# Optimization experiments

Hardware: AMD Instinct MI355X
Metric: run time of the kernel (lower is better)

Reference implementation:

```python
import jax, jax.numpy as jnp
import numpy as np

B, L, E = 64, 256, 512
H = 1024          # hidden_size
N = 128           # memory_size
HS = 64           # head_size (memory width)
NH = 4            # NTM heads
OUT = 1024        # output_size
TNH = 4           # transformer nhead
IN_DIM = E + NH * HS          # 768
POD = H + NH * HS             # 1280


def ln(x, g, b, eps=1e-5):
    mu = x.mean(-1, keepdims=True)
    v = ((x - mu) ** 2).mean(-1, keepdims=True)
    return (x - mu) / jnp.sqrt(v + eps) * g + b


def setup_inputs() -> dict:
    key = jax.random.key(0)
    ks = iter(jax.random.split(key, 64))
    def w(shape, s=0.05):
        return jax.random.normal(next(ks), shape, jnp.float32) * s
    f32 = jnp.float32
    return dict(
        x_emb=jax.random.normal(next(ks), (B, L, E), f32),
        in_g=jnp.ones(IN_DIM, f32), in_b=jnp.zeros(IN_DIM, f32),
        W_ih=w((4 * H, IN_DIM)), W_hh=w((4 * H, H)),
        b_ih=jnp.zeros(4 * H, f32), b_hh=jnp.zeros(4 * H, f32),
        cn_g=jnp.ones(H, f32), cn_b=jnp.zeros(H, f32),
        W_rk=w((NH * HS, H)), b_rk=jnp.zeros(NH * HS, f32),
        W_wk=w((NH * HS, H)), b_wk=jnp.zeros(NH * HS, f32),
        W_ws=w((NH, H)), b_ws=jnp.zeros(NH, f32),
        W_ev=w((NH * HS, H)), b_ev=jnp.zeros(NH * HS, f32),
        attn_w=w((3 * HS, HS)), attn_b=jnp.zeros(3 * HS, f32),
        attn_ow=w((HS, HS)), attn_ob=jnp.zeros(HS, f32),
        l1_w=w((2 * HS, HS)), l1_b=jnp.zeros(2 * HS, f32),
        l2_w=w((HS, 2 * HS)), l2_b=jnp.zeros(HS, f32),
        tn1_g=jnp.ones(HS, f32), tn1_b=jnp.zeros(HS, f32),
        tn2_g=jnp.ones(HS, f32), tn2_b=jnp.zeros(HS, f32),
        rkn_g=jnp.ones(HS, f32), rkn_b=jnp.zeros(HS, f32),
        wkn_g=jnp.ones(HS, f32), wkn_b=jnp.zeros(HS, f32),
        mn_g=jnp.ones(HS, f32), mn_b=jnp.zeros(HS, f32),
        po_g=jnp.ones(POD, f32), po_b=jnp.zeros(POD, f32),
        W_proj=w((OUT, POD)), b_proj=jnp.zeros(OUT, f32),
    )


def reference(x_emb, in_g, in_b, W_ih, W_hh, b_ih, b_hh, cn_g, cn_b,
              W_rk, b_rk, W_wk, b_wk, W_ws, b_ws, W_ev, b_ev,
              attn_w, attn_b, attn_ow, attn_ob, l1_w, l1_b, l2_w, l2_b,
              tn1_g, tn1_b, tn2_g, tn2_b, rkn_g, rkn_b, wkn_g, wkn_b,
              mn_g, mn_b, po_g, po_b, W_proj, b_proj):
    Bc = x_emb.shape[0]
    dh = HS // TNH

    def tblock(mem):  # [B, N, HS], eval-mode (dropout = identity)
        qkv = mem @ attn_w.T + attn_b
        q, k, v = jnp.split(qkv, 3, axis=-1)
        q = q.reshape(Bc, N, TNH, dh)
        k = k.reshape(Bc, N, TNH, dh)
        v = v.reshape(Bc, N, TNH, dh)
        a = jax.nn.softmax(jnp.einsum('bqhd,bkhd->bhqk', q, k) / jnp.sqrt(jnp.float32(dh)), axis=-1)
        o = jnp.einsum('bhqk,bkhd->bqhd', a, v).reshape(Bc, N, HS)
        o = o @ attn_ow.T + attn_ob
        x = ln(mem + o, tn1_g, tn1_b)
        ff = jax.nn.gelu(x @ l1_w.T + l1_b, approximate=False) @ l2_w.T + l2_b
        return ln(x + ff, tn2_g, tn2_b)

    def step(carry, x_t):
        h, c, mem, rc = carry
        inp = ln(jnp.concatenate([x_t, rc.reshape(Bc, -1)], axis=-1), in_g, in_b)
        gates = inp @ W_ih.T + b_ih + h @ W_hh.T + b_hh  # torch gate order i,f,g,o
        i, f, g, o = jnp.split(gates, 4, axis=-1)
        c = jax.nn.sigmoid(f) * c + jax.nn.sigmoid(i) * jnp.tanh(g)
        h = jax.nn.sigmoid(o) * jnp.tanh(c)
        hn = ln(h, cn_g, cn_b)
        rk = (hn @ W_rk.T + b_rk).reshape(Bc, NH, HS)
        wk = (hn @ W_wk.T + b_wk).reshape(Bc, NH, HS)
        ws = jax.nn.sigmoid(hn @ W_ws.T + b_ws)                    # [B, NH]
        ev = jax.nn.sigmoid(hn @ W_ev.T + b_ev).reshape(Bc, NH, HS)
        # addressing
        mem = tblock(mem)
        mem_n = ln(mem, mn_g, mn_b)
        rk = ln(rk, rkn_g, rkn_b)
        wk = ln(wk, wkn_g, wkn_b)
        rw = jax.nn.softmax(jnp.einsum('bnk,bmk->bnm', rk, mem_n), axis=-1)
        rc = jnp.einsum('bnm,bmh->bnh', rw, mem)
        ww = jax.nn.softmax(jnp.einsum('bnk,bmk->bnm', wk, mem_n), axis=-1)
        erase = jnp.einsum('bnm,bnh->bmh', ww, ev)
        mem = mem * (1.0 - erase)
        add = jnp.einsum('bnm,bnh->bmh', ww, ws[..., None] * wk)
        mem = mem + add
        out = ln(jnp.concatenate([hn, rc.reshape(Bc, -1)], axis=-1), po_g, po_b)
        logits = out @ W_proj.T + b_proj
        return (h, c, mem, rc), logits

    h0 = jnp.zeros((Bc, H), x_emb.dtype)
    c0 = jnp.zeros((Bc, H), x_emb.dtype)
    mem0 = jnp.zeros((Bc, N, HS), x_emb.dtype)
    rc0 = jnp.zeros((Bc, NH, HS), x_emb.dtype)
    (h, c, mem, _), outs = jax.lax.scan(step, (h0, c0, mem0, rc0), jnp.swapaxes(x_emb, 0, 1))
    return jnp.swapaxes(outs, 0, 1), mem, (h[None], c[None])
```

## Files before the change

### kernel.cpp

```cpp
#include <hip/hip_runtime.h>
#include <math.h>

typedef short s8v __attribute__((ext_vector_type(8)));
typedef float f32x4 __attribute__((ext_vector_type(4)));

__device__ inline float sigm(float x) { return 1.0f / (1.0f + expf(-x)); }
__device__ inline float dot4(const float4 a, const float4 b) {
  return a.x*b.x + a.y*b.y + a.z*b.z + a.w*b.w;
}
__device__ inline float wsum(float v) {
#pragma unroll
  for (int o = 32; o > 0; o >>= 1) v += __shfl_xor(v, o, 64);
  return v;
}
__device__ inline short f2bf(float f) {
  unsigned int u = __float_as_uint(f);
  unsigned int r = u + 0x7FFFu + ((u >> 16) & 1u);
  return (short)(r >> 16);
}
__device__ inline float bf2f(short h) {
  return __uint_as_float(((unsigned int)(unsigned short)h) << 16);
}
__device__ inline void storesplit(float v, short* __restrict__ hi,
                                  short* __restrict__ lo, size_t idx) {
  short h = f2bf(v);
  hi[idx] = h;
  lo[idx] = f2bf(v - bf2f(h));
}

template<int LD, int KS>
__device__ __forceinline__ void gemm4(const short* __restrict__ A,
                                      const short* __restrict__ B,
                                      f32x4 acc[4], int lane) {
  int off = (lane & 15) * LD + ((lane >> 4) * 8);
#pragma unroll 4
  for (int kb = 0; kb < KS; kb++) {
    int ko = off + kb*32;
    s8v bb = *(const s8v*)(B + ko);
#pragma unroll
    for (int m = 0; m < 4; m++) {
      s8v aa = *(const s8v*)(A + ko + m*16*LD);
      acc[m] = __builtin_amdgcn_mfma_f32_16x16x32_bf16(aa, bb, acc[m], 0,0,0);
    }
  }
}

__global__ void kprep_g(const float* __restrict__ Wih, const float* __restrict__ Whh,
                        short* __restrict__ WgH, short* __restrict__ WgL) {
  int r = blockIdx.y, k = blockIdx.x*256 + threadIdx.x;
  if (k < 1792) {
    int jt = r >> 6, rr = r & 63, ul = rr >> 2, gi = rr & 3;
    int orow = gi*1024 + jt*16 + ul;
    float v = (k < 768) ? Wih[(size_t)orow*768 + k] : Whh[(size_t)orow*1024 + (k-768)];
    storesplit(v, WgH, WgL, (size_t)r*1792 + k);
  }
}
__global__ void kprep_p(const float* __restrict__ Wp, short* __restrict__ W) {
  int j = blockIdx.y, k = blockIdx.x*256 + threadIdx.x;
  W[(size_t)j*1280 + k] = f2bf(Wp[(size_t)j*1280 + k]);
}
__global__ void kprep_h(const float* __restrict__ Wrk, const float* __restrict__ Wwk,
                        const float* __restrict__ Wev, const float* __restrict__ Wws,
                        short* __restrict__ WhH, short* __restrict__ WhL) {
  int j = blockIdx.y, k = blockIdx.x*256 + threadIdx.x;
  float v;
  if (j < 256)      v = Wrk[(size_t)j*1024 + k];
  else if (j < 512) v = Wwk[(size_t)(j-256)*1024 + k];
  else if (j < 768) v = Wev[(size_t)(j-512)*1024 + k];
  else if (j < 772) v = Wws[(size_t)(j-768)*1024 + k];
  else v = 0.f;
  storesplit(v, WhH, WhL, (size_t)j*1024 + k);
}
__global__ void kprep_q(const float* __restrict__ aw, short* __restrict__ WH,
                        short* __restrict__ WL) {
  int i = blockIdx.x*64 + threadIdx.x;
  storesplit(aw[i], WH, WL, i);
}

__global__ __launch_bounds__(256) void k_prep0(
    const float* __restrict__ x_emb, const float* __restrict__ in_g,
    const float* __restrict__ in_b, short* __restrict__ inbH,
    short* __restrict__ inbL)
{
  __shared__ float rs[4], rq[4];
  int b = blockIdx.x, tid = threadIdx.x, lane = tid & 63, wid = tid >> 6;
  float v3[3]; float s = 0.f, sq = 0.f;
#pragma unroll
  for (int i = 0; i < 3; i++) {
    int k = tid + i * 256;
    float v = (k < 512) ? x_emb[(size_t)b * 256 * 512 + k] : 0.f;
    v3[i] = v; s += v; sq += v * v;
  }
  s = wsum(s); sq = wsum(sq);
  if (lane == 0) { rs[wid] = s; rq[wid] = sq; }
  __syncthreads();
  float ts = rs[0]+rs[1]+rs[2]+rs[3], tq = rq[0]+rq[1]+rq[2]+rq[3];
  float mu = ts / 768.f, var = tq / 768.f - mu * mu;
  float rstd = rsqrtf(var + 1e-5f);
#pragma unroll
  for (int i = 0; i < 3; i++) {
    int k = tid + i * 256;
    storesplit((v3[i] - mu) * rstd * in_g[k] + in_b[k], inbH, inbL, b*1792 + k);
  }
}

__global__ __launch_bounds__(256) void kA(
    const short* __restrict__ inbH, const short* __restrict__ inbL,
    short* __restrict__ inbHn, short* __restrict__ inbLn,
    const short* __restrict__ WgH, const short* __restrict__ WgL,
    const float* __restrict__ b_ih, const float* __restrict__ b_hh,
    float* __restrict__ cbuf, float* __restrict__ hbuf,
    float* __restrict__ hstat, float* __restrict__ gatesP,
    unsigned* __restrict__ tick,
    const short* __restrict__ membH, const short* __restrict__ membL,
    const short* __restrict__ WqH, const short* __restrict__ WqL,
    const float* __restrict__ attn_b,
    const short* __restrict__ pob16, const short* __restrict__ Wp16,
    const float* __restrict__ b_proj,
    float* __restrict__ qkv, float* __restrict__ outs, int t)
{
  __shared__ char poolA[40960];
  __shared__ unsigned sOld;
  int bid = blockIdx.x, tid = threadIdx.x, lane = tid & 63, w = tid >> 6;
  if (bid < 128) {
    if (t >= 256) return;
    short (*sT)[4][2560] = (short(*)[4][2560])poolA;
    int jt = bid & 63, kt = bid >> 6;
    int k0 = kt * 896;
    int srow = tid >> 2, scol = (tid & 3) * 8;
    const short* gAH = inbH + srow*1792 + k0 + scol;
    const short* gAL = inbL + srow*1792 + k0 + scol;
    const short* gBH = WgH + (size_t)(jt*64 + srow)*1792 + k0 + scol;
    const short* gBL = WgL + (size_t)(jt*64 + srow)*1792 + k0 + scol;
    int4 rAH = *(const int4*)gAH, rAL = *(const int4*)gAL;
    int4 rBH = *(const int4*)gBH, rBL = *(const int4*)gBL;
    *(int4*)&sT[0][0][srow*40 + scol] = rAH;
    *(int4*)&sT[0][1][srow*40 + scol] = rAL;
    *(int4*)&sT[0][2][srow*40 + scol] = rBH;
    *(int4*)&sT[0][3][srow*40 + scol] = rBL;
    f32x4 acc[4] = {};
    int arow = lane & 15, akk = (lane >> 4) * 8;
    for (int c = 0; c < 28; ++c) {
      int cur = c & 1;
      if (c < 27) {
        rAH = *(const int4*)(gAH + (c+1)*32);
        rAL = *(const int4*)(gAL + (c+1)*32);
        rBH = *(const int4*)(gBH + (c+1)*32);
        rBL = *(const int4*)(gBL + (c+1)*32);
      }
      __syncthreads();
      s8v bh = *(const s8v*)&sT[cur][2][(w*16 + arow)*40 + akk];
      s8v bl = *(const s8v*)&sT[cur][3][(w*16 + arow)*40 + akk];
#pragma unroll
      for (int ms = 0; ms < 4; ++ms) {
        s8v ah = *(const s8v*)&sT[cur][0][(arow + ms*16)*40 + akk];
        s8v al = *(const s8v*)&sT[cur][1][(arow + ms*16)*40 + akk];
        acc[ms] = __builtin_amdgcn_mfma_f32_16x16x32_bf16(ah, bh, acc[ms], 0,0,0);
        acc[ms] = __builtin_amdgcn_mfma_f32_16x16x32_bf16(al, bh, acc[ms], 0,0,0);
        acc[ms] = __builtin_amdgcn_mfma_f32_16x16x32_bf16(ah, bl, acc[ms], 0,0,0);
      }
      if (c < 27) {
        *(int4*)&sT[cur^1][0][srow*40 + scol] = rAH;
        *(int4*)&sT[cur^1][1][srow*40 + scol] = rAL;
        *(int4*)&sT[cur^1][2][srow*40 + scol] = rBH;
        *(int4*)&sT[cur^1][3][srow*40 + scol] = rBL;
      }
    }
    {
      float* gp = gatesP + (size_t)kt * 262144;
      int j = jt*64 + w*16 + (lane & 15);
#pragma unroll
      for (int ms = 0; ms < 4; ms++)
#pragma unroll
        for (int r = 0; r < 4; r++) {
          int b = ms*16 + (lane>>4)*4 + r;
          gp[b*4096 + j] = acc[ms][r];
        }
    }
    __syncthreads();
    if (tid == 0) {
      __threadfence();
      sOld = __hip_atomic_fetch_add(&tick[jt], 1u, __ATOMIC_ACQ_REL,
                                    __HIP_MEMORY_SCOPE_AGENT);
    }
    __syncthreads();
    if (!(sOld & 1u)) return;
    {
      const float* pp = gatesP + (size_t)(kt^1) * 262144;
      int j = jt*64 + w*16 + (lane & 15);
#pragma unroll
      for (int ms = 0; ms < 4; ms++)
#pragma unroll
        for (int r = 0; r < 4; r++) {
          int b = ms*16 + (lane>>4)*4 + r;
          acc[ms][r] += __hip_atomic_load(&pp[b*4096 + j], __ATOMIC_RELAXED,
                                          __HIP_MEMORY_SCOPE_AGENT);
        }
    }
    float* sC = (float*)poolA;
    float* sRed = (float*)(poolA + 17408);
    __syncthreads();
    {
      int rr = w*16 + (lane & 15);
#pragma unroll
      for (int ms = 0; ms < 4; ms++)
#pragma unroll
        for (int r = 0; r < 4; r++) {
          int b = ms*16 + (lane>>4)*4 + r;
          sC[b*68 + rr] = acc[ms][r];
        }
    }
    __syncthreads();
    {
      int b = tid & 63;
      float sh = 0.f, sh2 = 0.f;
#pragma unroll
      for (int q = 0; q < 4; q++) {
        int ul = (tid >> 6) + q*4;
        int u = jt*16 + ul;
        float gi_ = sC[b*68 + ul*4 + 0] + b_ih[u]        + b_hh[u];
        float gf  = sC[b*68 + ul*4 + 1] + b_ih[1024 + u] + b_hh[1024 + u];
        float gg  = sC[b*68 + ul*4 + 2] + b_ih[2048 + u] + b_hh[2048 + u];
        float go  = sC[b*68 + ul*4 + 3] + b_ih[3072 + u] + b_hh[3072 + u];
        float cn = sigm(gf)*cbuf[b*1024 + u] + sigm(gi_)*tanhf(gg);
        float hh = sigm(go)*tanhf(cn);
        cbuf[b*1024 + u] = cn;
        hbuf[b*1024 + u] = hh;
        storesplit(hh, inbHn, inbLn, b*1792 + 768 + u);
        sh += hh; sh2 += hh*hh;
      }
      sRed[(tid>>6)*64 + b] = sh;
      sRed[256 + (tid>>6)*64 + b] = sh2;
    }
    __syncthreads();
    if (tid < 64) {
      float s0 = sRed[tid]+sRed[64+tid]+sRed[128+tid]+sRed[192+tid];
      float s1 = sRed[256+tid]+sRed[320+tid]+sRed[384+tid]+sRed[448+tid];
      hstat[(tid*64 + jt)*2]     = s0;
      hstat[(tid*64 + jt)*2 + 1] = s1;
    }
  } else if (bid < 192) {
    if (t >= 256) return;
    int b = bid - 128;
    const short* Ah = membH + (size_t)b * 8192;
    const short* Al = membL + (size_t)b * 8192;
    int ao = (w*32 + (lane & 15)) * 64 + (lane >> 4) * 8;
    s8v ah00 = *(const s8v*)(Ah + ao);
    s8v ah01 = *(const s8v*)(Ah + ao + 32);
    s8v ah10 = *(const s8v*)(Ah + ao + 16*64);
    s8v ah11 = *(const s8v*)(Ah + ao + 16*64 + 32);
    s8v al00 = *(const s8v*)(Al + ao);
    s8v al01 = *(const s8v*)(Al + ao + 32);
    s8v al10 = *(const s8v*)(Al + ao + 16*64);
    s8v al11 = *(const s8v*)(Al + ao + 16*64 + 32);
    int bo = (lane & 15) * 64 + (lane >> 4) * 8;
    for (int n = 0; n < 12; n++) {
      s8v bh0 = *(const s8v*)(WqH + bo + n*1024);
      s8v bh1 = *(const s8v*)(WqH + bo + n*1024 + 32);
      s8v bl0 = *(const s8v*)(WqL + bo + n*1024);
      s8v bl1 = *(const s8v*)(WqL + bo + n*1024 + 32);
      f32x4 acc0 = {}, acc1 = {};
      acc0 = __builtin_amdgcn_mfma_f32_16x16x32_bf16(ah00, bh0, acc0, 0,0,0);
      acc0 = __builtin_amdgcn_mfma_f32_16x16x32_bf16(ah01, bh1, acc0, 0,0,0);
      acc0 = __builtin_amdgcn_mfma_f32_16x16x32_bf16(al00, bh0, acc0, 0,0,0);
      acc0 = __builtin_amdgcn_mfma_f32_16x16x32_bf16(al01, bh1, acc0, 0,0,0);
      acc0 = __builtin_amdgcn_mfma_f32_16x16x32_bf16(ah00, bl0, acc0, 0,0,0);
      acc0 = __builtin_amdgcn_mfma_f32_16x16x32_bf16(ah01, bl1, acc0, 0,0,0);
      acc1 = __builtin_amdgcn_mfma_f32_16x16x32_bf16(ah10, bh0, acc1, 0,0,0);
      acc1 = __builtin_amdgcn_mfma_f32_16x16x32_bf16(ah11, bh1, acc1, 0,0,0);
      acc1 = __builtin_amdgcn_mfma_f32_16x16x32_bf16(al10, bh0, acc1, 0,0,0);
      acc1 = __builtin_amdgcn_mfma_f32_16x16x32_bf16(al11, bh1, acc1, 0,0,0);
      acc1 = __builtin_amdgcn_mfma_f32_16x16x32_bf16(ah10, bl0, acc1, 0,0,0);
      acc1 = __builtin_amdgcn_mfma_f32_16x16x32_bf16(ah11, bl1, acc1, 0,0,0);
      int j = n*16 + (lane & 15);
      int ch = j >> 6, jj = j & 63;
      float bv = attn_b[j];
#pragma unroll
      for (int r = 0; r < 4; r++) {
        int m0 = w*32 + (lane>>4)*4 + r;
        qkv[((size_t)(b*3 + ch)*128 + m0)*64 + jj] = acc0[r] + bv;
        qkv[((size_t)(b*3 + ch)*128 + m0 + 16)*64 + jj] = acc1[r] + bv;
      }
    }
  } else {
    if (t == 0) return;
    int jt = bid - 192;
    f32x4 acc[4] = {};
    const short* B = Wp16 + (size_t)(jt*64 + w*16) * 1280;
    gemm4<1280, 40>(pob16, B, acc, lane);
    int j = jt*64 + w*16 + (lane & 15);
    float bv = b_proj[j];
#pragma unroll
    for (int ms = 0; ms < 4; ms++)
#pragma unroll
      for (int r = 0; r < 4; r++) {
        int b = ms*16 + (lane>>4)*4 + r;
        outs[((size_t)b*256 + (t-1))*1024 + j] = acc[ms][r] + bv;
      }
  }
}

__global__ __launch_bounds__(512) void kB(
    float* __restrict__ mem, const float* __restrict__ qkv,
    const float* __restrict__ attn_ow, const float* __restrict__ attn_ob,
    const float* __restrict__ l1w, const float* __restrict__ l1b,
    const float* __restrict__ l2w, const float* __restrict__ l2b,
    const float* __restrict__ tn1g, const float* __restrict__ tn1b,
    const float* __restrict__ tn2g, const float* __restrict__ tn2b,
    const float* __restrict__ hbuf, const float* __restrict__ hstat,
    const float* __restrict__ cn_g, const float* __restrict__ cn_b,
    const short* __restrict__ WhH, const short* __restrict__ WhL,
    float* __restrict__ hp)
{
  __shared__ float pool[35200];
  int bid = blockIdx.x, tid = threadIdx.x;
  int lane = tid & 63, wid = tid >> 6;
  if (bid < 52) {
    int kt = bid & 3, jt = bid >> 2;
    {
      int b2 = tid & 63, part = tid >> 6;
      float s0 = 0.f, s1 = 0.f;
#pragma unroll 4
      for (int m2 = 0; m2 < 8; m2++) {
        int jt2 = part*8 + m2;
        s0 += hstat[(b2*64 + jt2)*2];
        s1 += hstat[(b2*64 + jt2)*2 + 1];
      }
      pool[part*64 + b2] = s0;
      pool[512 + part*64 + b2] = s1;
    }
    __syncthreads();
    if (tid < 64) {
      float ts = 0.f, tq = 0.f;
#pragma unroll
      for (int p2 = 0; p2 < 8; p2++) {
        ts += pool[p2*64 + tid];
        tq += pool[512 + p2*64 + tid];
      }
      float mu = ts / 1024.f;
      pool[1024+tid] = mu;
      pool[1088+tid] = rsqrtf(tq/1024.f - mu*mu + 1e-5f);
    }
    __syncthreads();
    short* sAH = (short*)&pool[1152];
    short* sAL = sAH + 2560;
    int srow = tid >> 3, scol = (tid & 7) * 4;
    int arow = lane & 15, akk = (lane >> 4) * 8;
    f32x4 acc[4] = {};
    for (int c = 0; c < 8; ++c) {
      __syncthreads();
      {
        float mu = pool[1024 + srow], rsd = pool[1088 + srow];
        int kbase = kt*256 + c*32 + scol;
        const float* hpt = hbuf + srow*1024 + kbase;
#pragma unroll
        for (int i = 0; i < 4; i++) {
          float hnv = (hpt[i] - mu) * rsd * cn_g[kbase + i] + cn_b[kbase + i];
          short hh = f2bf(hnv);
          sAH[srow*40 + scol + i] = hh;
          sAL[srow*40 + scol + i] = f2bf(hnv - bf2f(hh));
        }
      }
      __syncthreads();
      if (wid < 4) {
        size_t bo = (size_t)(jt*64 + wid*16 + arow)*1024 + kt*256 + c*32 + akk;
        s8v bh = *(const s8v*)(WhH + bo);
        s8v bl = *(const s8v*)(WhL + bo);
#pragma unroll
        for (int ms = 0; ms < 4; ++ms) {
          s8v ah = *(const s8v*)&sAH[(arow + ms*16)*40 + akk];
          s8v al = *(const s8v*)&sAL[(arow + ms*16)*40 + akk];
          acc[ms] = __builtin_amdgcn_mfma_f32_16x16x32_bf16(ah, bh, acc[ms], 0,0,0);
          acc[ms] = __builtin_amdgcn_mfma_f32_16x16x32_bf16(al, bh, acc[ms], 0,0,0);
          acc[ms] = __builtin_amdgcn_mfma_f32_16x16x32_bf16(ah, bl, acc[ms], 0,0,0);
        }
      }
    }
    if (wid < 4) {
      int j = jt*64 + wid*16 + (lane & 15);
#pragma unroll
      for (int ms = 0; ms < 4; ms++)
#pragma unroll
        for (int r = 0; r < 4; r++) {
          int b2 = ms*16 + (lane>>4)*4 + r;
          hp[(size_t)kt*53248 + b2*832 + j] = acc[ms][r];
        }
    }
    return;
  }
  float* sK  = pool;
  float* sV  = pool + 8704;
  float* sX  = pool + 17408;
  float* sM  = pool + 19584;
  float* sO  = pool + 21760;
  float* sS  = pool + 23936;
  float* sRed= pool + 34176;
  int bb0 = bid - 52;
  int b = bb0 & 63, mt = bb0 >> 6;
  int m0 = mt * 32;
  const float* qb = qkv + (size_t)b*3*8192;
  for (int i = tid*4; i < 8192; i += 2048) {
    *(float4*)&sK[i] = *(const float4*)&qb[8192 + i];
    *(float4*)&sV[i] = *(const float4*)&qb[16384 + i];
  }
  {
    int i = tid*4;
    int m = i >> 6, s = i & 63;
    *(float4*)&sX[m*68+s] = *(const float4*)&qb[m0*64 + i];
    *(float4*)&sM[m*68+s] = *(const float4*)&mem[(size_t)b*8192 + m0*64 + i];
  }
  __syncthreads();
  int m = tid >> 4, hd = (tid >> 2) & 3, q = tid & 3;
  const float* qp = sX + m*68 + hd*16;
  float4 q0 = *(const float4*)(qp),   q1 = *(const float4*)(qp+4);
  float4 q2 = *(const float4*)(qp+8), q3 = *(const float4*)(qp+12);
  int kmb = q * 32;
  float mx = -1e30f;
#pragma unroll 4
  for (int kk = 0; kk < 32; kk++) {
    const float* kp = sK + (kmb+kk)*64 + hd*16;
    float sc = dot4(q0, *(const float4*)kp)     + dot4(q1, *(const float4*)(kp+4))
             + dot4(q2, *(const float4*)(kp+8)) + dot4(q3, *(const float4*)(kp+12));
    mx = fmaxf(mx, sc * 0.25f);
  }
  float4 o0 = {0,0,0,0}, o1 = {0,0,0,0}, o2 = {0,0,0,0}, o3 = {0,0,0,0};
  float sum = 0.f;
#pragma unroll 4
  for (int kk = 0; kk < 32; kk++) {
    const float* kp = sK + (kmb+kk)*64 + hd*16;
    float sc = dot4(q0, *(const float4*)kp)     + dot4(q1, *(const float4*)(kp+4))
             + dot4(q2, *(const float4*)(kp+8)) + dot4(q3, *(const float4*)(kp+12));
    float e = expf(sc * 0.25f - mx);
    sum += e;
    const float* vp = sV + (kmb+kk)*64 + hd*16;
    float4 v0 = *(const float4*)vp,     v1 = *(const float4*)(vp+4);
    float4 v2 = *(const float4*)(vp+8), v3 = *(const float4*)(vp+12);
    o0.x += e*v0.x; o0.y += e*v0.y; o0.z += e*v0.z; o0.w += e*v0.w;
    o1.x += e*v1.x; o1.y += e*v1.y; o1.z += e*v1.z; o1.w += e*v1.w;
    o2.x += e*v2.x; o2.y += e*v2.y; o2.z += e*v2.z; o2.w += e*v2.w;
    o3.x += e*v3.x; o3.y += e*v3.y; o3.z += e*v3.z; o3.w += e*v3.w;
  }
  {
    float* pp = sS + tid*20;
    *(float4*)&pp[0]  = o0; *(float4*)&pp[4]  = o1;
    *(float4*)&pp[8]  = o2; *(float4*)&pp[12] = o3;
    sRed[tid] = mx; sRed[512+tid] = sum;
  }
  __syncthreads();
  if (q == 0) {
    float m1 = sRed[tid+1], m2 = sRed[tid+2], m3 = sRed[tid+3];
    float M = fmaxf(fmaxf(mx, m1), fmaxf(m2, m3));
    float e0 = expf(mx - M), e1 = expf(m1 - M), e2 = expf(m2 - M), e3 = expf(m3 - M);
    float inv = 1.0f / (sum*e0 + sRed[512+tid+1]*e1 + sRed[512+tid+2]*e2
                        + sRed[512+tid+3]*e3);
    const float* p1 = sS + (tid+1)*20;
    const float* p2 = sS + (tid+2)*20;
    const float* p3 = sS + (tid+3)*20;
    float oo[16];
    *(float4*)&oo[0] = o0; *(float4*)&oo[4] = o1;
    *(float4*)&oo[8] = o2; *(float4*)&oo[12] = o3;
    float* op = sO + m*68 + hd*16;
#pragma unroll
    for (int d = 0; d < 16; d++)
      op[d] = (oo[d]*e0 + p1[d]*e1 + p2[d]*e2 + p3[d]*e3) * inv;
  }
  __syncthreads();
  for (int idx = tid; idx < 4096; idx += 512) {
    int j = idx >> 6, s = idx & 63;
    sS[j*68 + s] = attn_ow[idx];
  }
  __syncthreads();
  {
    int mm = tid >> 4, jset = tid & 15;
    float4 orow[16];
#pragma unroll
    for (int r = 0; r < 16; r++) orow[r] = *(const float4*)&sO[mm*68 + r*4];
#pragma unroll
    for (int i = 0; i < 4; i++) {
      int j = jset + 16*i;
      const float* wr = sS + j*68;
      float acc = attn_ob[j];
#pragma unroll
      for (int r = 0; r < 16; r++) acc += dot4(orow[r], *(const float4*)&wr[r*4]);
      sM[mm*68 + j] += acc;
    }
  }
  __syncthreads();
  for (int r = wid; r < 32; r += 8) {
    float v = sM[r*68 + lane];
    float ssum = wsum(v), ssq = wsum(v*v);
    float mu = ssum*(1.f/64), var = ssq*(1.f/64) - mu*mu;
    sX[r*68+lane] = (v - mu)*rsqrtf(var+1e-5f)*tn1g[lane] + tn1b[lane];
  }
  for (int idx = tid; idx < 8192; idx += 512) {
    int f = idx >> 6, s = idx & 63;
    sK[f*68 + s] = l1w[idx];
  }
  for (int idx = tid; idx < 8192; idx += 512) {
    int j = idx >> 7, s = idx & 127;
    sV[j*132 + s] = l2w[idx];
  }
  __syncthreads();
  {
    int mm = tid >> 4, fs = tid & 15;
    float4 xr[16];
#pragma unroll
    for (int r = 0; r < 16; r++) xr[r] = *(const float4*)&sX[mm*68 + r*4];
#pragma unroll 4
    for (int i = 0; i < 8; i++) {
      int f = fs + 16*i;
      const float* wr = sK + f*68;
      float acc = l1b[f];
#pragma unroll
      for (int r = 0; r < 16; r++) acc += dot4(xr[r], *(const float4*)&wr[r*4]);
      sS[mm*132 + f] = 0.5f*acc*(1.0f + erff(acc*0.70710678118654752f));
    }
  }
  __syncthreads();
  {
    int mm = tid >> 4, jset = tid & 15;
    float acc6[4];
#pragma unroll
    for (int i = 0; i < 4; i++) acc6[i] = sX[mm*68 + jset + 16*i] + l2b[jset + 16*i];
#pragma unroll
    for (int h = 0; h < 2; h++) {
      float4 fr[16];
#pragma unroll
      for (int r = 0; r < 16; r++) fr[r] = *(const float4*)&sS[mm*132 + h*64 + r*4];
#pragma unroll
      for (int i = 0; i < 4; i++) {
        int j = jset + 16*i;
        const float* wr = sV + j*132 + h*64;
        float a = 0.f;
#pragma unroll
        for (int r = 0; r < 16; r++) a += dot4(fr[r], *(const float4*)&wr[r*4]);
        acc6[i] += a;
      }
    }
#pragma unroll
    for (int i = 0; i < 4; i++) sO[mm*68 + jset + 16*i] = acc6[i];
  }
  __syncthreads();
  for (int r = wid; r < 32; r += 8) {
    float v = sO[r*68 + lane];
    float ssum = wsum(v), ssq = wsum(v*v);
    float mu = ssum*(1.f/64), var = ssq*(1.f/64) - mu*mu;
    mem[(size_t)b*8192 + (m0+r)*64 + lane] =
        (v - mu)*rsqrtf(var+1e-5f)*tn2g[lane] + tn2b[lane];
  }
}

__global__ __launch_bounds__(256) void kC(
    float* __restrict__ mem, short* __restrict__ membH, short* __restrict__ membL,
    const float* __restrict__ hp, const float* __restrict__ hstat,
    const float* __restrict__ hbuf,
    const float* __restrict__ b_rk, const float* __restrict__ b_wk,
    const float* __restrict__ b_ev, const float* __restrict__ b_ws,
    const float* __restrict__ rkn_g, const float* __restrict__ rkn_b,
    const float* __restrict__ wkn_g, const float* __restrict__ wkn_b,
    const float* __restrict__ cn_g, const float* __restrict__ cn_b,
    const float* __restrict__ mng, const float* __restrict__ mnb,
    const float* __restrict__ pog, const float* __restrict__ pob,
    const float* __restrict__ x_emb, const float* __restrict__ in_g,
    const float* __restrict__ in_b,
    short* __restrict__ inbHn, short* __restrict__ inbLn,
    short* __restrict__ pob16, int tnext)
{
  __shared__ float sMT[8192];
  __shared__ float sMN[128*65];
  __shared__ float sRk[256], sWk[256], sEv[256], sWs[4];
  __shared__ float sRw[512], sWw[512], sRc[256];
  __shared__ float rs[4], rq[4];
  __shared__ float sHst[2];
  int b = blockIdx.x, tid = threadIdx.x, lane = tid & 63, wid = tid >> 6;
  for (int i = tid*4; i < 8192; i += 1024)
    *(float4*)&sMT[i] = *(const float4*)&mem[(size_t)b*8192 + i];
  {
    const float* h0 = hp + (size_t)b*832;
    const float* h1 = hp + 53248 + (size_t)b*832;
    const float* h2 = hp + 2*53248 + (size_t)b*832;
    const float* h3 = hp + 3*53248 + (size_t)b*832;
    float v = h0[tid] + h1[tid] + h2[tid] + h3[tid] + b_rk[tid];
    float ssum = wsum(v), ssq = wsum(v*v);
    float mu = ssum*(1.f/64), var = ssq*(1.f/64) - mu*mu;
    sRk[tid] = (v - mu)*rsqrtf(var+1e-5f)*rkn_g[lane] + rkn_b[lane];
    v = h0[256+tid] + h1[256+tid] + h2[256+tid] + h3[256+tid] + b_wk[tid];
    ssum = wsum(v); ssq = wsum(v*v);
    mu = ssum*(1.f/64); var = ssq*(1.f/64) - mu*mu;
    sWk[tid] = (v - mu)*rsqrtf(var+1e-5f)*wkn_g[lane] + wkn_b[lane];
    sEv[tid] = sigm(h0[512+tid] + h1[512+tid] + h2[512+tid] + h3[512+tid] + b_ev[tid]);
    if (tid < 4)
      sWs[tid] = sigm(h0[768+tid] + h1[768+tid] + h2[768+tid] + h3[768+tid] + b_ws[tid]);
  }
  if (wid == 0) {
    float v0 = hstat[(b*64 + lane)*2], v1 = hstat[(b*64 + lane)*2 + 1];
    float s0 = wsum(v0), s1 = wsum(v1);
    if (lane == 0) {
      float mu = s0 / 1024.f;
      sHst[0] = mu;
      sHst[1] = rsqrtf(s1/1024.f - mu*mu + 1e-5f);
    }
  }
  __syncthreads();
  for (int r = wid; r < 128; r += 4) {
    float v = sMT[r*64 + lane];
    float ssum = wsum(v), ssq = wsum(v*v);
    float mu = ssum*(1.f/64), var = ssq*(1.f/64) - mu*mu;
    sMN[r*65 + lane] = (v - mu)*rsqrtf(var+1e-5f)*mng[lane] + mnb[lane];
  }
  __syncthreads();
#pragma unroll
  for (int q = 0; q < 4; q++) {
    int idx = tid + q*256;
    int which = idx >> 9;
    int n = (idx >> 7) & 3, m = idx & 127;
    const float* key = (which ? sWk : sRk) + n*64;
    const float* mr = sMN + m*65;
    float acc = 0.f;
#pragma unroll 8
    for (int k = 0; k < 64; k++) acc += key[k]*mr[k];
    (which ? sWw : sRw)[n*128 + m] = acc;
  }
  __syncthreads();
  for (int r = wid; r < 8; r += 4) {
    float* row = (r < 4) ? (sRw + r*128) : (sWw + (r-4)*128);
    float a0 = row[lane], a1 = row[lane+64];
    float mx = fmaxf(a0, a1);
#pragma unroll
    for (int o = 32; o > 0; o >>= 1) mx = fmaxf(mx, __shfl_xor(mx, o, 64));
    float e0 = expf(a0 - mx), e1 = expf(a1 - mx);
    float inv = 1.0f / wsum(e0 + e1);
    row[lane] = e0*inv; row[lane+64] = e1*inv;
  }
  __syncthreads();
  {
    int n = tid >> 6, s2 = tid & 63;
    float acc = 0.f;
    for (int mm = 0; mm < 128; mm++) acc += sRw[n*128 + mm] * sMT[mm*64 + s2];
    sRc[tid] = acc;
  }
  __syncthreads();
  for (int idx = tid; idx < 8192; idx += 256) {
    int mm = idx >> 6, s2 = idx & 63;
    float er = 0.f, ad = 0.f;
#pragma unroll
    for (int n = 0; n < 4; n++) {
      float w = sWw[n*128 + mm];
      er += w * sEv[n*64 + s2];
      ad += w * sWs[n] * sWk[n*64 + s2];
    }
    float val = sMT[idx]*(1.0f - er) + ad;
    mem[(size_t)b*8192 + idx] = val;
    storesplit(val, membH, membL, (size_t)b*8192 + idx);
  }
  float hmu = sHst[0], hrs = sHst[1];
  float v5[5]; float s = 0.f, sq = 0.f;
#pragma unroll
  for (int i = 0; i < 5; i++) {
    int k = tid + i*256;
    float v = (k < 1024)
      ? (hbuf[b*1024 + k] - hmu)*hrs*cn_g[k] + cn_b[k]
      : sRc[k-1024];
    v5[i] = v; s += v; sq += v*v;
  }
  s = wsum(s); sq = wsum(sq);
  if (lane == 0) { rs[wid] = s; rq[wid] = sq; }
  __syncthreads();
  {
    float ts = rs[0]+rs[1]+rs[2]+rs[3], tq = rq[0]+rq[1]+rq[2]+rq[3];
    float mu = ts/1280.f, var = tq/1280.f - mu*mu;
    float rstd = rsqrtf(var + 1e-5f);
#pragma unroll
    for (int i = 0; i < 5; i++) {
      int k = tid + i*256;
      pob16[b*1280 + k] = f2bf((v5[i] - mu)*rstd*pog[k] + pob[k]);
    }
  }
  if (tnext < 256) {
    __syncthreads();
    float v3[3]; float s2 = 0.f, q2 = 0.f;
#pragma unroll
    for (int i = 0; i < 3; i++) {
      int k = tid + i*256;
      float v = (k < 512) ? x_emb[((size_t)b*256 + tnext)*512 + k] : sRc[k-512];
      v3[i] = v; s2 += v; q2 += v*v;
    }
    s2 = wsum(s2); q2 = wsum(q2);
    if (lane == 0) { rs[wid] = s2; rq[wid] = q2; }
    __syncthreads();
    float ts = rs[0]+rs[1]+rs[2]+rs[3], tq = rq[0]+rq[1]+rq[2]+rq[3];
    float mu = ts/768.f, var = tq/768.f - mu*mu;
    float rstd = rsqrtf(var + 1e-5f);
#pragma unroll
    for (int i = 0; i < 3; i++) {
      int k = tid + i*256;
      storesplit((v3[i] - mu)*rstd*in_g[k] + in_b[k], inbHn, inbLn, b*1792 + k);
    }
  }
}

__global__ void k_final(const float* __restrict__ mem, const float* __restrict__ hbuf,
                        const float* __restrict__ cbuf, float* __restrict__ out)
{
  int i = blockIdx.x * 256 + threadIdx.x;
  if (i < 524288) out[16777216 + i] = mem[i];
  if (i < 65536) {
    out[17301504 + i] = hbuf[i];
    out[17367040 + i] = cbuf[i];
  }
}

extern "C" void kernel_launch(void* const* d_in, const int* in_sizes, int n_in,
                              void* d_out, int out_size, void* d_ws, size_t ws_size,
                              hipStream_t stream) {
  const float* x_emb  = (const float*)d_in[0];
  const float* in_g   = (const float*)d_in[1];
  const float* in_b   = (const float*)d_in[2];
  const float* W_ih   = (const float*)d_in[3];
  const float* W_hh   = (const float*)d_in[4];
  const float* b_ih   = (const float*)d_in[5];
  const float* b_hh   = (const float*)d_in[6];
  const float* cn_g   = (const float*)d_in[7];
  const float* cn_b   = (const float*)d_in[8];
  const float* W_rk   = (const float*)d_in[9];
  const float* b_rk   = (const float*)d_in[10];
  const float* W_wk   = (const float*)d_in[11];
  const float* b_wk   = (const float*)d_in[12];
  const float* W_ws   = (const float*)d_in[13];
  const float* b_ws   = (const float*)d_in[14];
  const float* W_ev   = (const float*)d_in[15];
  const float* b_ev   = (const float*)d_in[16];
  const float* attn_w = (const float*)d_in[17];
  const float* attn_b = (const float*)d_in[18];
  const float* attn_ow= (const float*)d_in[19];
  const float* attn_ob= (const float*)d_in[20];
  const float* l1_w   = (const float*)d_in[21];
  const float* l1_b   = (const float*)d_in[22];
  const float* l2_w   = (const float*)d_in[23];
  const float* l2_b   = (const float*)d_in[24];
  const float* tn1_g  = (const float*)d_in[25];
  const float* tn1_b  = (const float*)d_in[26];
  const float* tn2_g  = (const float*)d_in[27];
  const float* tn2_b  = (const float*)d_in[28];
  const float* rkn_g  = (const float*)d_in[29];
  const float* rkn_b  = (const float*)d_in[30];
  const float* wkn_g  = (const float*)d_in[31];
  const float* wkn_b  = (const float*)d_in[32];
  const float* mn_g   = (const float*)d_in[33];
  const float* mn_b   = (const float*)d_in[34];
  const float* po_g   = (const float*)d_in[35];
  const float* po_b   = (const float*)d_in[36];
  const float* W_proj = (const float*)d_in[37];
  const float* b_proj = (const float*)d_in[38];

  float* ws = (float*)d_ws;
  float* mem    = ws;
  float* cbuf   = ws + 524288;
  float* hbuf   = ws + 589824;
  float* gatesP = ws + 655360;
  float* hp     = ws + 1179648;
  float* hstat  = ws + 1392640;
  unsigned* tick = (unsigned*)(ws + 1400832);
  float* qkvb   = ws + 1400896;
  short* sb     = (short*)(ws + 2973760);
  short* inbH0 = sb;
  short* inbL0 = sb + 114688;
  short* inbH1 = sb + 229376;
  short* inbL1 = sb + 344064;
  short* membH = sb + 458752;
  short* membL = sb + 983040;
  short* pob16 = sb + 1507328;
  short* WgH   = sb + 1589248;
  short* WgL   = sb + 8929280;
  short* WhH   = sb + 16269312;
  short* WhL   = sb + 17121280;
  short* WqH   = sb + 17973248;
  short* WqL   = sb + 17985536;
  short* Wp16  = sb + 17997824;

  hipMemsetAsync(ws, 0, 655360 * sizeof(float), stream);
  hipMemsetAsync(tick, 0, 256, stream);
  hipMemsetAsync(sb, 0, 1507328 * sizeof(short), stream);

  kprep_g<<<dim3(7, 4096), 256, 0, stream>>>(W_ih, W_hh, WgH, WgL);
  kprep_p<<<dim3(5, 1024), 256, 0, stream>>>(W_proj, Wp16);
  kprep_h<<<dim3(4, 832), 256, 0, stream>>>(W_rk, W_wk, W_ev, W_ws, WhH, WhL);
  kprep_q<<<dim3(192), 64, 0, stream>>>(attn_w, WqH, WqL);
  k_prep0<<<64, 256, 0, stream>>>(x_emb, in_g, in_b, inbH0, inbL0);

  float* outs = (float*)d_out;
  short* bufsH[2] = {inbH0, inbH1};
  short* bufsL[2] = {inbL0, inbL1};
  for (int t = 0; t < 256; t++) {
    kA<<<208, 256, 0, stream>>>(bufsH[t&1], bufsL[t&1], bufsH[(t+1)&1], bufsL[(t+1)&1],
                                WgH, WgL, b_ih, b_hh, cbuf, hbuf, hstat, gatesP, tick,
                                membH, membL, WqH, WqL, attn_b,
                                pob16, Wp16, b_proj, qkvb, outs, t);
    kB<<<308, 512, 0, stream>>>(mem, qkvb, attn_ow, attn_ob,
                                l1_w, l1_b, l2_w, l2_b,
                                tn1_g, tn1_b, tn2_g, tn2_b,
                                hbuf, hstat, cn_g, cn_b, WhH, WhL, hp);
    kC<<<64, 256, 0, stream>>>(mem, membH, membL, hp, hstat, hbuf,
                               b_rk, b_wk, b_ev, b_ws,
                               rkn_g, rkn_b, wkn_g, wkn_b, cn_g, cn_b,
                               mn_g, mn_b, po_g, po_b,
                               x_emb, in_g, in_b,
                               bufsH[(t+1)&1], bufsL[(t+1)&1], pob16, t+1);
  }
  kA<<<208, 256, 0, stream>>>(bufsH[0], bufsL[0], bufsH[1], bufsL[1],
                              WgH, WgL, b_ih, b_hh, cbuf, hbuf, hstat, gatesP, tick,
                              membH, membL, WqH, WqL, attn_b,
                              pob16, Wp16, b_proj, qkvb, outs, 256);
  k_final<<<2048, 256, 0, stream>>>(mem, hbuf, cbuf, (float*)d_out);
}
```

Measured before the change: 27.37 ms.

## Restructure step pipeline from three kernels to two, fusing transformer block into LSTM kernel

The per-timestep schedule now uses two kernels instead of three. The transformer block over memory moves into spare blocks of the LSTM/projection kernel, and the QKV projection moves into the addressing kernel, which computes it from the freshly updated memory held in shared memory. The LSTM gate GEMM now splits K across two halves of a 512-thread block and reduces through shared memory, replacing the cross-block atomic tick and global partial buffer. Head projections now read fp32 weights directly in kC rather than the pre-split bf16 copies. This removes one launch per step and the global membH/membL round trip, at the cost of heavier, more register-hungry fused blocks and fewer blocks doing the gate GEMM.

```diff
diff --git a/kernel.cpp b/kernel.cpp
--- a/kernel.cpp
+++ b/kernel.cpp
@@ -59,18 +59,6 @@
   int j = blockIdx.y, k = blockIdx.x*256 + threadIdx.x;
   W[(size_t)j*1280 + k] = f2bf(Wp[(size_t)j*1280 + k]);
 }
-__global__ void kprep_h(const float* __restrict__ Wrk, const float* __restrict__ Wwk,
-                        const float* __restrict__ Wev, const float* __restrict__ Wws,
-                        short* __restrict__ WhH, short* __restrict__ WhL) {
-  int j = blockIdx.y, k = blockIdx.x*256 + threadIdx.x;
-  float v;
-  if (j < 256)      v = Wrk[(size_t)j*1024 + k];
-  else if (j < 512) v = Wwk[(size_t)(j-256)*1024 + k];
-  else if (j < 768) v = Wev[(size_t)(j-512)*1024 + k];
-  else if (j < 772) v = Wws[(size_t)(j-768)*1024 + k];
-  else v = 0.f;
-  storesplit(v, WhH, WhL, (size_t)j*1024 + k);
-}
 __global__ void kprep_q(const float* __restrict__ aw, short* __restrict__ WH,
                         short* __restrict__ WL) {
   int i = blockIdx.x*64 + threadIdx.x;
@@ -104,30 +92,44 @@
   }
 }
 
-__global__ __launch_bounds__(256) void kA(
+__global__ __launch_bounds__(256) void k_prepq0(
+    const float* __restrict__ attn_b, float* __restrict__ qkv)
+{
+  int b = blockIdx.x, tid = threadIdx.x;
+  for (int i = tid; i < 24576; i += 256) {
+    int ch = i >> 13, j = i & 63;
+    qkv[(size_t)b*24576 + i] = attn_b[ch*64 + j];
+  }
+}
+
+__global__ __launch_bounds__(512) void kA(
     const short* __restrict__ inbH, const short* __restrict__ inbL,
     short* __restrict__ inbHn, short* __restrict__ inbLn,
     const short* __restrict__ WgH, const short* __restrict__ WgL,
     const float* __restrict__ b_ih, const float* __restrict__ b_hh,
     float* __restrict__ cbuf, float* __restrict__ hbuf,
-    float* __restrict__ hstat, float* __restrict__ gatesP,
-    unsigned* __restrict__ tick,
-    const short* __restrict__ membH, const short* __restrict__ membL,
-    const short* __restrict__ WqH, const short* __restrict__ WqL,
-    const float* __restrict__ attn_b,
+    float* __restrict__ hstat,
+    const float* __restrict__ qkv, float* __restrict__ mem,
+    const float* __restrict__ attn_ow, const float* __restrict__ attn_ob,
+    const float* __restrict__ l1w, const float* __restrict__ l1b,
+    const float* __restrict__ l2w, const float* __restrict__ l2b,
+    const float* __restrict__ tn1g, const float* __restrict__ tn1b,
+    const float* __restrict__ tn2g, const float* __restrict__ tn2b,
     const short* __restrict__ pob16, const short* __restrict__ Wp16,
-    const float* __restrict__ b_proj,
-    float* __restrict__ qkv, float* __restrict__ outs, int t)
+    const float* __restrict__ b_proj, float* __restrict__ outs, int t)
 {
-  __shared__ char poolA[40960];
-  __shared__ unsigned sOld;
-  int bid = blockIdx.x, tid = threadIdx.x, lane = tid & 63, w = tid >> 6;
-  if (bid < 128) {
+  __shared__ float pool[35200];
+  int bid = blockIdx.x, tid = threadIdx.x;
+  int lane = tid & 63;
+  if (bid < 64) {
     if (t >= 256) return;
-    short (*sT)[4][2560] = (short(*)[4][2560])poolA;
-    int jt = bid & 63, kt = bid >> 6;
+    int jt = bid;
+    int kt = tid >> 8;
+    int tl = tid & 255;
+    int w4 = (tid >> 6) & 3;
+    short (*sT)[4][2560] = (short(*)[4][2560])((char*)pool + kt*40960);
     int k0 = kt * 896;
-    int srow = tid >> 2, scol = (tid & 3) * 8;
+    int srow = tl >> 2, scol = (tl & 3) * 8;
     const short* gAH = inbH + srow*1792 + k0 + scol;
     const short* gAL = inbL + srow*1792 + k0 + scol;
     const short* gBH = WgH + (size_t)(jt*64 + srow)*1792 + k0 + scol;
@@ -149,8 +151,8 @@
         rBL = *(const int4*)(gBL + (c+1)*32);
       }
       __syncthreads();
-      s8v bh = *(const s8v*)&sT[cur][2][(w*16 + arow)*40 + akk];
-      s8v bl = *(const s8v*)&sT[cur][3][(w*16 + arow)*40 + akk];
+      s8v bh = *(const s8v*)&sT[cur][2][(w4*16 + arow)*40 + akk];
+      s8v bl = *(const s8v*)&sT[cur][3][(w4*16 + arow)*40 + akk];
 #pragma unroll
       for (int ms = 0; ms < 4; ++ms) {
         s8v ah = *(const s8v*)&sT[cur][0][(arow + ms*16)*40 + akk];
@@ -166,62 +168,32 @@
         *(int4*)&sT[cur^1][3][srow*40 + scol] = rBL;
       }
     }
+    __syncthreads();
+    float* sC = pool;
+    float* sRed = pool + 8704;
     {
-      float* gp = gatesP + (size_t)kt * 262144;
-      int j = jt*64 + w*16 + (lane & 15);
+      float* sCk = sC + kt*4352;
+      int rr = w4*16 + (lane & 15);
 #pragma unroll
       for (int ms = 0; ms < 4; ms++)
 #pragma unroll
         for (int r = 0; r < 4; r++) {
           int b = ms*16 + (lane>>4)*4 + r;
-          gp[b*4096 + j] = acc[ms][r];
+          sCk[b*68 + rr] = acc[ms][r];
         }
     }
-    __syncthreads();
-    if (tid == 0) {
-      __threadfence();
-      sOld = __hip_atomic_fetch_add(&tick[jt], 1u, __ATOMIC_ACQ_REL,
-                                    __HIP_MEMORY_SCOPE_AGENT);
-    }
-    __syncthreads();
-    if (!(sOld & 1u)) return;
-    {
-      const float* pp = gatesP + (size_t)(kt^1) * 262144;
-      int j = jt*64 + w*16 + (lane & 15);
-#pragma unroll
-      for (int ms = 0; ms < 4; ms++)
-#pragma unroll
-        for (int r = 0; r < 4; r++) {
-          int b = ms*16 + (lane>>4)*4 + r;
-          acc[ms][r] += __hip_atomic_load(&pp[b*4096 + j], __ATOMIC_RELAXED,
-                                          __HIP_MEMORY_SCOPE_AGENT);
-        }
-    }
-    float* sC = (float*)poolA;
-    float* sRed = (float*)(poolA + 17408);
     __syncthreads();
     {
-      int rr = w*16 + (lane & 15);
-#pragma unroll
-      for (int ms = 0; ms < 4; ms++)
-#pragma unroll
-        for (int r = 0; r < 4; r++) {
-          int b = ms*16 + (lane>>4)*4 + r;
-          sC[b*68 + rr] = acc[ms][r];
-        }
-    }
-    __syncthreads();
-    {
-      int b = tid & 63;
+      int b = tid & 63, ug = tid >> 6;
       float sh = 0.f, sh2 = 0.f;
 #pragma unroll
-      for (int q = 0; q < 4; q++) {
-        int ul = (tid >> 6) + q*4;
+      for (int q = 0; q < 2; q++) {
+        int ul = ug*2 + q;
         int u = jt*16 + ul;
-        float gi_ = sC[b*68 + ul*4 + 0] + b_ih[u]        + b_hh[u];
-        float gf  = sC[b*68 + ul*4 + 1] + b_ih[1024 + u] + b_hh[1024 + u];
-        float gg  = sC[b*68 + ul*4 + 2] + b_ih[2048 + u] + b_hh[2048 + u];
-        float go  = sC[b*68 + ul*4 + 3] + b_ih[3072 + u] + b_hh[3072 + u];
+        float gi_ = sC[b*68 + ul*4 + 0] + sC[4352 + b*68 + ul*4 + 0] + b_ih[u]        + b_hh[u];
+        float gf  = sC[b*68 + ul*4 + 1] + sC[4352 + b*68 + ul*4 + 1] + b_ih[1024 + u] + b_hh[1024 + u];
+        float gg  = sC[b*68 + ul*4 + 2] + sC[4352 + b*68 + ul*4 + 2] + b_ih[2048 + u] + b_hh[2048 + u];
+        float go  = sC[b*68 + ul*4 + 3] + sC[4352 + b*68 + ul*4 + 3] + b_ih[3072 + u] + b_hh[3072 + u];
         float cn = sigm(gf)*cbuf[b*1024 + u] + sigm(gi_)*tanhf(gg);
         float hh = sigm(go)*tanhf(cn);
         cbuf[b*1024 + u] = cn;
@@ -229,66 +201,191 @@
         storesplit(hh, inbHn, inbLn, b*1792 + 768 + u);
         sh += hh; sh2 += hh*hh;
       }
-      sRed[(tid>>6)*64 + b] = sh;
-      sRed[256 + (tid>>6)*64 + b] = sh2;
+      sRed[ug*64 + b] = sh;
+      sRed[512 + ug*64 + b] = sh2;
     }
     __syncthreads();
     if (tid < 64) {
-      float s0 = sRed[tid]+sRed[64+tid]+sRed[128+tid]+sRed[192+tid];
-      float s1 = sRed[256+tid]+sRed[320+tid]+sRed[384+tid]+sRed[448+tid];
+      float s0 = 0.f, s1 = 0.f;
+#pragma unroll
+      for (int p = 0; p < 8; p++) { s0 += sRed[p*64 + tid]; s1 += sRed[512 + p*64 + tid]; }
       hstat[(tid*64 + jt)*2]     = s0;
       hstat[(tid*64 + jt)*2 + 1] = s1;
     }
   } else if (bid < 192) {
     if (t >= 256) return;
-    int b = bid - 128;
-    const short* Ah = membH + (size_t)b * 8192;
-    const short* Al = membL + (size_t)b * 8192;
-    int ao = (w*32 + (lane & 15)) * 64 + (lane >> 4) * 8;
-    s8v ah00 = *(const s8v*)(Ah + ao);
-    s8v ah01 = *(const s8v*)(Ah + ao + 32);
-    s8v ah10 = *(const s8v*)(Ah + ao + 16*64);
-    s8v ah11 = *(const s8v*)(Ah + ao + 16*64 + 32);
-    s8v al00 = *(const s8v*)(Al + ao);
-    s8v al01 = *(const s8v*)(Al + ao + 32);
-    s8v al10 = *(const s8v*)(Al + ao + 16*64);
-    s8v al11 = *(const s8v*)(Al + ao + 16*64 + 32);
-    int bo = (lane & 15) * 64 + (lane >> 4) * 8;
-    for (int n = 0; n < 12; n++) {
-      s8v bh0 = *(const s8v*)(WqH + bo + n*1024);
-      s8v bh1 = *(const s8v*)(WqH + bo + n*1024 + 32);
-      s8v bl0 = *(const s8v*)(WqL + bo + n*1024);
-      s8v bl1 = *(const s8v*)(WqL + bo + n*1024 + 32);
-      f32x4 acc0 = {}, acc1 = {};
-      acc0 = __builtin_amdgcn_mfma_f32_16x16x32_bf16(ah00, bh0, acc0, 0,0,0);
-      acc0 = __builtin_amdgcn_mfma_f32_16x16x32_bf16(ah01, bh1, acc0, 0,0,0);
-      acc0 = __builtin_amdgcn_mfma_f32_16x16x32_bf16(al00, bh0, acc0, 0,0,0);
-      acc0 = __builtin_amdgcn_mfma_f32_16x16x32_bf16(al01, bh1, acc0, 0,0,0);
-      acc0 = __builtin_amdgcn_mfma_f32_16x16x32_bf16(ah00, bl0, acc0, 0,0,0);
-      acc0 = __builtin_amdgcn_mfma_f32_16x16x32_bf16(ah01, bl1, acc0, 0,0,0);
-      acc1 = __builtin_amdgcn_mfma_f32_16x16x32_bf16(ah10, bh0, acc1, 0,0,0);
-      acc1 = __builtin_amdgcn_mfma_f32_16x16x32_bf16(ah11, bh1, acc1, 0,0,0);
-      acc1 = __builtin_amdgcn_mfma_f32_16x16x32_bf16(al10, bh0, acc1, 0,0,0);
-      acc1 = __builtin_amdgcn_mfma_f32_16x16x32_bf16(al11, bh1, acc1, 0,0,0);
-      acc1 = __builtin_amdgcn_mfma_f32_16x16x32_bf16(ah10, bl0, acc1, 0,0,0);
-      acc1 = __builtin_amdgcn_mfma_f32_16x16x32_bf16(ah11, bl1, acc1, 0,0,0);
-      int j = n*16 + (lane & 15);
-      int ch = j >> 6, jj = j & 63;
-      float bv = attn_b[j];
-#pragma unroll
-      for (int r = 0; r < 4; r++) {
-        int m0 = w*32 + (lane>>4)*4 + r;
-        qkv[((size_t)(b*3 + ch)*128 + m0)*64 + jj] = acc0[r] + bv;
-        qkv[((size_t)(b*3 + ch)*128 + m0 + 16)*64 + jj] = acc1[r] + bv;
-      }
+    float* sK  = pool;
+    float* sV  = pool + 8704;
+    float* sX  = pool + 17408;
+    float* sM  = pool + 19584;
+    float* sO  = pool + 21760;
+    float* sS  = pool + 23936;
+    float* sRed= pool + 34176;
+    int pb = bid - 64;
+    int b = pb & 63, pr = pb >> 6;
+    int wid = tid >> 6;
+    const float* qb = qkv + (size_t)b*3*8192;
+    for (int it = 0; it < 2; ++it) {
+      int m0 = (pr*2 + it) * 32;
+      for (int i = tid*4; i < 8192; i += 2048) {
+        *(float4*)&sK[i] = *(const float4*)&qb[8192 + i];
+        *(float4*)&sV[i] = *(const float4*)&qb[16384 + i];
+      }
+      {
+        int i = tid*4;
+        int m = i >> 6, s = i & 63;
+        *(float4*)&sX[m*68+s] = *(const float4*)&qb[m0*64 + i];
+        *(float4*)&sM[m*68+s] = *(const float4*)&mem[(size_t)b*8192 + m0*64 + i];
+      }
+      __syncthreads();
+      int m = tid >> 4, hd = (tid >> 2) & 3, q = tid & 3;
+      const float* qp = sX + m*68 + hd*16;
+      float4 q0 = *(const float4*)(qp),   q1 = *(const float4*)(qp+4);
+      float4 q2 = *(const float4*)(qp+8), q3 = *(const float4*)(qp+12);
+      int kmb = q * 32;
+      float mx = -1e30f;
+#pragma unroll 4
+      for (int kk = 0; kk < 32; kk++) {
+        const float* kp = sK + (kmb+kk)*64 + hd*16;
+        float sc = dot4(q0, *(const float4*)kp)     + dot4(q1, *(const float4*)(kp+4))
+                 + dot4(q2, *(const float4*)(kp+8)) + dot4(q3, *(const float4*)(kp+12));
+        mx = fmaxf(mx, sc * 0.25f);
+      }
+      float4 o0 = {0,0,0,0}, o1 = {0,0,0,0}, o2 = {0,0,0,0}, o3 = {0,0,0,0};
+      float sum = 0.f;
+#pragma unroll 4
+      for (int kk = 0; kk < 32; kk++) {
+        const float* kp = sK + (kmb+kk)*64 + hd*16;
+        float sc = dot4(q0, *(const float4*)kp)     + dot4(q1, *(const float4*)(kp+4))
+                 + dot4(q2, *(const float4*)(kp+8)) + dot4(q3, *(const float4*)(kp+12));
+        float e = expf(sc * 0.25f - mx);
+        sum += e;
+        const float* vp = sV + (kmb+kk)*64 + hd*16;
+        float4 v0 = *(const float4*)vp,     v1 = *(const float4*)(vp+4);
+        float4 v2 = *(const float4*)(vp+8), v3 = *(const float4*)(vp+12);
+        o0.x += e*v0.x; o0.y += e*v0.y; o0.z += e*v0.z; o0.w += e*v0.w;
+        o1.x += e*v1.x; o1.y += e*v1.y; o1.z += e*v1.z; o1.w += e*v1.w;
+        o2.x += e*v2.x; o2.y += e*v2.y; o2.z += e*v2.z; o2.w += e*v2.w;
+        o3.x += e*v3.x; o3.y += e*v3.y; o3.z += e*v3.z; o3.w += e*v3.w;
+      }
+      {
+        float* pp = sS + tid*20;
+        *(float4*)&pp[0]  = o0; *(float4*)&pp[4]  = o1;
+        *(float4*)&pp[8]  = o2; *(float4*)&pp[12] = o3;
+        sRed[tid] = mx; sRed[512+tid] = sum;
+      }
+      __syncthreads();
+      if (q == 0) {
+        float m1 = sRed[tid+1], m2 = sRed[tid+2], m3 = sRed[tid+3];
+        float M = fmaxf(fmaxf(mx, m1), fmaxf(m2, m3));
+        float e0 = expf(mx - M), e1 = expf(m1 - M), e2 = expf(m2 - M), e3 = expf(m3 - M);
+        float inv = 1.0f / (sum*e0 + sRed[512+tid+1]*e1 + sRed[512+tid+2]*e2
+                            + sRed[512+tid+3]*e3);
+        const float* p1 = sS + (tid+1)*20;
+        const float* p2 = sS + (tid+2)*20;
+        const float* p3 = sS + (tid+3)*20;
+        float oo[16];
+        *(float4*)&oo[0] = o0; *(float4*)&oo[4] = o1;
+        *(float4*)&oo[8] = o2; *(float4*)&oo[12] = o3;
+        float* op = sO + m*68 + hd*16;
+#pragma unroll
+        for (int d = 0; d < 16; d++)
+          op[d] = (oo[d]*e0 + p1[d]*e1 + p2[d]*e2 + p3[d]*e3) * inv;
+      }
+      __syncthreads();
+      for (int idx = tid; idx < 4096; idx += 512) {
+        int j = idx >> 6, s = idx & 63;
+        sS[j*68 + s] = attn_ow[idx];
+      }
+      __syncthreads();
+      {
+        int mm = tid >> 4, jset = tid & 15;
+        float4 orow[16];
+#pragma unroll
+        for (int r = 0; r < 16; r++) orow[r] = *(const float4*)&sO[mm*68 + r*4];
+#pragma unroll
+        for (int i = 0; i < 4; i++) {
+          int j = jset + 16*i;
+          const float* wr = sS + j*68;
+          float acc = attn_ob[j];
+#pragma unroll
+          for (int r = 0; r < 16; r++) acc += dot4(orow[r], *(const float4*)&wr[r*4]);
+          sM[mm*68 + j] += acc;
+        }
+      }
+      __syncthreads();
+      for (int r = wid; r < 32; r += 8) {
+        float v = sM[r*68 + lane];
+        float ssum = wsum(v), ssq = wsum(v*v);
+        float mu = ssum*(1.f/64), var = ssq*(1.f/64) - mu*mu;
+        sX[r*68+lane] = (v - mu)*rsqrtf(var+1e-5f)*tn1g[lane] + tn1b[lane];
+      }
+      for (int idx = tid; idx < 8192; idx += 512) {
+        int f = idx >> 6, s = idx & 63;
+        sK[f*68 + s] = l1w[idx];
+      }
+      for (int idx = tid; idx < 8192; idx += 512) {
+        int j = idx >> 7, s = idx & 127;
+        sV[j*132 + s] = l2w[idx];
+      }
+      __syncthreads();
+      {
+        int mm = tid >> 4, fs = tid & 15;
+        float4 xr[16];
+#pragma unroll
+        for (int r = 0; r < 16; r++) xr[r] = *(const float4*)&sX[mm*68 + r*4];
+#pragma unroll 4
+        for (int i = 0; i < 8; i++) {
+          int f = fs + 16*i;
+          const float* wr = sK + f*68;
+          float acc = l1b[f];
+#pragma unroll
+          for (int r = 0; r < 16; r++) acc += dot4(xr[r], *(const float4*)&wr[r*4]);
+          sS[mm*132 + f] = 0.5f*acc*(1.0f + erff(acc*0.70710678118654752f));
+        }
+      }
+      __syncthreads();
+      {
+        int mm = tid >> 4, jset = tid & 15;
+        float acc6[4];
+#pragma unroll
+        for (int i = 0; i < 4; i++) acc6[i] = sX[mm*68 + jset + 16*i] + l2b[jset + 16*i];
+#pragma unroll
+        for (int h = 0; h < 2; h++) {
+          float4 fr[16];
+#pragma unroll
+          for (int r = 0; r < 16; r++) fr[r] = *(const float4*)&sS[mm*132 + h*64 + r*4];
+#pragma unroll
+          for (int i = 0; i < 4; i++) {
+            int j = jset + 16*i;
+            const float* wr = sV + j*132 + h*64;
+            float a = 0.f;
+#pragma unroll
+            for (int r = 0; r < 16; r++) a += dot4(fr[r], *(const float4*)&wr[r*4]);
+            acc6[i] += a;
+          }
+        }
+#pragma unroll
+        for (int i = 0; i < 4; i++) sO[mm*68 + jset + 16*i] = acc6[i];
+      }
+      __syncthreads();
+      for (int r = wid; r < 32; r += 8) {
+        float v = sO[r*68 + lane];
+        float ssum = wsum(v), ssq = wsum(v*v);
+        float mu = ssum*(1.f/64), var = ssq*(1.f/64) - mu*mu;
+        mem[(size_t)b*8192 + (m0+r)*64 + lane] =
+            (v - mu)*rsqrtf(var+1e-5f)*tn2g[lane] + tn2b[lane];
+      }
+      __syncthreads();
     }
   } else {
     if (t == 0) return;
     int jt = bid - 192;
+    int w = tid >> 6;
     f32x4 acc[4] = {};
-    const short* B = Wp16 + (size_t)(jt*64 + w*16) * 1280;
+    const short* B = Wp16 + (size_t)(jt*128 + w*16) * 1280;
     gemm4<1280, 40>(pob16, B, acc, lane);
-    int j = jt*64 + w*16 + (lane & 15);
+    int j = jt*128 + w*16 + (lane & 15);
     float bv = b_proj[j];
 #pragma unroll
     for (int ms = 0; ms < 4; ms++)
@@ -300,299 +397,46 @@
   }
 }
 
-__global__ __launch_bounds__(512) void kB(
-    float* __restrict__ mem, const float* __restrict__ qkv,
-    const float* __restrict__ attn_ow, const float* __restrict__ attn_ob,
-    const float* __restrict__ l1w, const float* __restrict__ l1b,
-    const float* __restrict__ l2w, const float* __restrict__ l2b,
-    const float* __restrict__ tn1g, const float* __restrict__ tn1b,
-    const float* __restrict__ tn2g, const float* __restrict__ tn2b,
-    const float* __restrict__ hbuf, const float* __restrict__ hstat,
+__global__ __launch_bounds__(512) void kC(
+    float* __restrict__ mem, const float* __restrict__ hstat,
+    const float* __restrict__ hbuf,
     const float* __restrict__ cn_g, const float* __restrict__ cn_b,
-    const short* __restrict__ WhH, const short* __restrict__ WhL,
-    float* __restrict__ hp)
-{
-  __shared__ float pool[35200];
-  int bid = blockIdx.x, tid = threadIdx.x;
-  int lane = tid & 63, wid = tid >> 6;
-  if (bid < 52) {
-    int kt = bid & 3, jt = bid >> 2;
-    {
-      int b2 = tid & 63, part = tid >> 6;
-      float s0 = 0.f, s1 = 0.f;
-#pragma unroll 4
-      for (int m2 = 0; m2 < 8; m2++) {
-        int jt2 = part*8 + m2;
-        s0 += hstat[(b2*64 + jt2)*2];
-        s1 += hstat[(b2*64 + jt2)*2 + 1];
-      }
-      pool[part*64 + b2] = s0;
-      pool[512 + part*64 + b2] = s1;
-    }
-    __syncthreads();
-    if (tid < 64) {
-      float ts = 0.f, tq = 0.f;
-#pragma unroll
-      for (int p2 = 0; p2 < 8; p2++) {
-        ts += pool[p2*64 + tid];
-        tq += pool[512 + p2*64 + tid];
-      }
-      float mu = ts / 1024.f;
-      pool[1024+tid] = mu;
-      pool[1088+tid] = rsqrtf(tq/1024.f - mu*mu + 1e-5f);
-    }
-    __syncthreads();
-    short* sAH = (short*)&pool[1152];
-    short* sAL = sAH + 2560;
-    int srow = tid >> 3, scol = (tid & 7) * 4;
-    int arow = lane & 15, akk = (lane >> 4) * 8;
-    f32x4 acc[4] = {};
-    for (int c = 0; c < 8; ++c) {
-      __syncthreads();
-      {
-        float mu = pool[1024 + srow], rsd = pool[1088 + srow];
-        int kbase = kt*256 + c*32 + scol;
-        const float* hpt = hbuf + srow*1024 + kbase;
-#pragma unroll
-        for (int i = 0; i < 4; i++) {
-          float hnv = (hpt[i] - mu) * rsd * cn_g[kbase + i] + cn_b[kbase + i];
-          short hh = f2bf(hnv);
-          sAH[srow*40 + scol + i] = hh;
-          sAL[srow*40 + scol + i] = f2bf(hnv - bf2f(hh));
-        }
-      }
-      __syncthreads();
-      if (wid < 4) {
-        size_t bo = (size_t)(jt*64 + wid*16 + arow)*1024 + kt*256 + c*32 + akk;
-        s8v bh = *(const s8v*)(WhH + bo);
-        s8v bl = *(const s8v*)(WhL + bo);
-#pragma unroll
-        for (int ms = 0; ms < 4; ++ms) {
-          s8v ah = *(const s8v*)&sAH[(arow + ms*16)*40 + akk];
-          s8v al = *(const s8v*)&sAL[(arow + ms*16)*40 + akk];
-          acc[ms] = __builtin_amdgcn_mfma_f32_16x16x32_bf16(ah, bh, acc[ms], 0,0,0);
-          acc[ms] = __builtin_amdgcn_mfma_f32_16x16x32_bf16(al, bh, acc[ms], 0,0,0);
-          acc[ms] = __builtin_amdgcn_mfma_f32_16x16x32_bf16(ah, bl, acc[ms], 0,0,0);
-        }
-      }
-    }
-    if (wid < 4) {
-      int j = jt*64 + wid*16 + (lane & 15);
-#pragma unroll
-      for (int ms = 0; ms < 4; ms++)
-#pragma unroll
-        for (int r = 0; r < 4; r++) {
-          int b2 = ms*16 + (lane>>4)*4 + r;
-          hp[(size_t)kt*53248 + b2*832 + j] = acc[ms][r];
-        }
-    }
-    return;
-  }
-  float* sK  = pool;
-  float* sV  = pool + 8704;
-  float* sX  = pool + 17408;
-  float* sM  = pool + 19584;
-  float* sO  = pool + 21760;
-  float* sS  = pool + 23936;
-  float* sRed= pool + 34176;
-  int bb0 = bid - 52;
-  int b = bb0 & 63, mt = bb0 >> 6;
-  int m0 = mt * 32;
-  const float* qb = qkv + (size_t)b*3*8192;
-  for (int i = tid*4; i < 8192; i += 2048) {
-    *(float4*)&sK[i] = *(const float4*)&qb[8192 + i];
-    *(float4*)&sV[i] = *(const float4*)&qb[16384 + i];
-  }
-  {
-    int i = tid*4;
-    int m = i >> 6, s = i & 63;
-    *(float4*)&sX[m*68+s] = *(const float4*)&qb[m0*64 + i];
-    *(float4*)&sM[m*68+s] = *(const float4*)&mem[(size_t)b*8192 + m0*64 + i];
-  }
-  __syncthreads();
-  int m = tid >> 4, hd = (tid >> 2) & 3, q = tid & 3;
-  const float* qp = sX + m*68 + hd*16;
-  float4 q0 = *(const float4*)(qp),   q1 = *(const float4*)(qp+4);
-  float4 q2 = *(const float4*)(qp+8), q3 = *(const float4*)(qp+12);
-  int kmb = q * 32;
-  float mx = -1e30f;
-#pragma unroll 4
-  for (int kk = 0; kk < 32; kk++) {
-    const float* kp = sK + (kmb+kk)*64 + hd*16;
-    float sc = dot4(q0, *(const float4*)kp)     + dot4(q1, *(const float4*)(kp+4))
-             + dot4(q2, *(const float4*)(kp+8)) + dot4(q3, *(const float4*)(kp+12));
-    mx = fmaxf(mx, sc * 0.25f);
-  }
-  float4 o0 = {0,0,0,0}, o1 = {0,0,0,0}, o2 = {0,0,0,0}, o3 = {0,0,0,0};
-  float sum = 0.f;
-#pragma unroll 4
-  for (int kk = 0; kk < 32; kk++) {
-    const float* kp = sK + (kmb+kk)*64 + hd*16;
-    float sc = dot4(q0, *(const float4*)kp)     + dot4(q1, *(const float4*)(kp+4))
-             + dot4(q2, *(const float4*)(kp+8)) + dot4(q3, *(const float4*)(kp+12));
-    float e = expf(sc * 0.25f - mx);
-    sum += e;
-    const float* vp = sV + (kmb+kk)*64 + hd*16;
-    float4 v0 = *(const float4*)vp,     v1 = *(const float4*)(vp+4);
-    float4 v2 = *(const float4*)(vp+8), v3 = *(const float4*)(vp+12);
-    o0.x += e*v0.x; o0.y += e*v0.y; o0.z += e*v0.z; o0.w += e*v0.w;
-    o1.x += e*v1.x; o1.y += e*v1.y; o1.z += e*v1.z; o1.w += e*v1.w;
-    o2.x += e*v2.x; o2.y += e*v2.y; o2.z += e*v2.z; o2.w += e*v2.w;
-    o3.x += e*v3.x; o3.y += e*v3.y; o3.z += e*v3.z; o3.w += e*v3.w;
-  }
-  {
-    float* pp = sS + tid*20;
-    *(float4*)&pp[0]  = o0; *(float4*)&pp[4]  = o1;
-    *(float4*)&pp[8]  = o2; *(float4*)&pp[12] = o3;
-    sRed[tid] = mx; sRed[512+tid] = sum;
-  }
-  __syncthreads();
-  if (q == 0) {
-    float m1 = sRed[tid+1], m2 = sRed[tid+2], m3 = sRed[tid+3];
-    float M = fmaxf(fmaxf(mx, m1), fmaxf(m2, m3));
-    float e0 = expf(mx - M), e1 = expf(m1 - M), e2 = expf(m2 - M), e3 = expf(m3 - M);
-    float inv = 1.0f / (sum*e0 + sRed[512+tid+1]*e1 + sRed[512+tid+2]*e2
-                        + sRed[512+tid+3]*e3);
-    const float* p1 = sS + (tid+1)*20;
-    const float* p2 = sS + (tid+2)*20;
-    const float* p3 = sS + (tid+3)*20;
-    float oo[16];
-    *(float4*)&oo[0] = o0; *(float4*)&oo[4] = o1;
-    *(float4*)&oo[8] = o2; *(float4*)&oo[12] = o3;
-    float* op = sO + m*68 + hd*16;
-#pragma unroll
-    for (int d = 0; d < 16; d++)
-      op[d] = (oo[d]*e0 + p1[d]*e1 + p2[d]*e2 + p3[d]*e3) * inv;
-  }
-  __syncthreads();
-  for (int idx = tid; idx < 4096; idx += 512) {
-    int j = idx >> 6, s = idx & 63;
-    sS[j*68 + s] = attn_ow[idx];
-  }
-  __syncthreads();
-  {
-    int mm = tid >> 4, jset = tid & 15;
-    float4 orow[16];
-#pragma unroll
-    for (int r = 0; r < 16; r++) orow[r] = *(const float4*)&sO[mm*68 + r*4];
-#pragma unroll
-    for (int i = 0; i < 4; i++) {
-      int j = jset + 16*i;
-      const float* wr = sS + j*68;
-      float acc = attn_ob[j];
-#pragma unroll
-      for (int r = 0; r < 16; r++) acc += dot4(orow[r], *(const float4*)&wr[r*4]);
-      sM[mm*68 + j] += acc;
-    }
-  }
-  __syncthreads();
-  for (int r = wid; r < 32; r += 8) {
-    float v = sM[r*68 + lane];
-    float ssum = wsum(v), ssq = wsum(v*v);
-    float mu = ssum*(1.f/64), var = ssq*(1.f/64) - mu*mu;
-    sX[r*68+lane] = (v - mu)*rsqrtf(var+1e-5f)*tn1g[lane] + tn1b[lane];
-  }
-  for (int idx = tid; idx < 8192; idx += 512) {
-    int f = idx >> 6, s = idx & 63;
-    sK[f*68 + s] = l1w[idx];
-  }
-  for (int idx = tid; idx < 8192; idx += 512) {
-    int j = idx >> 7, s = idx & 127;
-    sV[j*132 + s] = l2w[idx];
-  }
-  __syncthreads();
-  {
-    int mm = tid >> 4, fs = tid & 15;
-    float4 xr[16];
-#pragma unroll
-    for (int r = 0; r < 16; r++) xr[r] = *(const float4*)&sX[mm*68 + r*4];
-#pragma unroll 4
-    for (int i = 0; i < 8; i++) {
-      int f = fs + 16*i;
-      const float* wr = sK + f*68;
-      float acc = l1b[f];
-#pragma unroll
-      for (int r = 0; r < 16; r++) acc += dot4(xr[r], *(const float4*)&wr[r*4]);
-      sS[mm*132 + f] = 0.5f*acc*(1.0f + erff(acc*0.70710678118654752f));
-    }
-  }
-  __syncthreads();
-  {
-    int mm = tid >> 4, jset = tid & 15;
-    float acc6[4];
-#pragma unroll
-    for (int i = 0; i < 4; i++) acc6[i] = sX[mm*68 + jset + 16*i] + l2b[jset + 16*i];
-#pragma unroll
-    for (int h = 0; h < 2; h++) {
-      float4 fr[16];
-#pragma unroll
-      for (int r = 0; r < 16; r++) fr[r] = *(const float4*)&sS[mm*132 + h*64 + r*4];
-#pragma unroll
-      for (int i = 0; i < 4; i++) {
-        int j = jset + 16*i;
-        const float* wr = sV + j*132 + h*64;
-        float a = 0.f;
-#pragma unroll
-        for (int r = 0; r < 16; r++) a += dot4(fr[r], *(const float4*)&wr[r*4]);
-        acc6[i] += a;
-      }
-    }
-#pragma unroll
-    for (int i = 0; i < 4; i++) sO[mm*68 + jset + 16*i] = acc6[i];
-  }
-  __syncthreads();
-  for (int r = wid; r < 32; r += 8) {
-    float v = sO[r*68 + lane];
-    float ssum = wsum(v), ssq = wsum(v*v);
-    float mu = ssum*(1.f/64), var = ssq*(1.f/64) - mu*mu;
-    mem[(size_t)b*8192 + (m0+r)*64 + lane] =
-        (v - mu)*rsqrtf(var+1e-5f)*tn2g[lane] + tn2b[lane];
-  }
-}
-
-__global__ __launch_bounds__(256) void kC(
-    float* __restrict__ mem, short* __restrict__ membH, short* __restrict__ membL,
-    const float* __restrict__ hp, const float* __restrict__ hstat,
-    const float* __restrict__ hbuf,
+    const float* __restrict__ W_rk, const float* __restrict__ W_wk,
+    const float* __restrict__ W_ev, const float* __restrict__ W_ws,
     const float* __restrict__ b_rk, const float* __restrict__ b_wk,
     const float* __restrict__ b_ev, const float* __restrict__ b_ws,
     const float* __restrict__ rkn_g, const float* __restrict__ rkn_b,
     const float* __restrict__ wkn_g, const float* __restrict__ wkn_b,
-    const float* __restrict__ cn_g, const float* __restrict__ cn_b,
     const float* __restrict__ mng, const float* __restrict__ mnb,
     const float* __restrict__ pog, const float* __restrict__ pob,
     const float* __restrict__ x_emb, const float* __restrict__ in_g,
     const float* __restrict__ in_b,
+    const short* __restrict__ WqH, const short* __restrict__ WqL,
+    const float* __restrict__ attn_b,
+    float* __restrict__ qkv,
     short* __restrict__ inbHn, short* __restrict__ inbLn,
     short* __restrict__ pob16, int tnext)
 {
-  __shared__ float sMT[8192];
-  __shared__ float sMN[128*65];
-  __shared__ float sRk[256], sWk[256], sEv[256], sWs[4];
-  __shared__ float sRw[512], sWw[512], sRc[256];
-  __shared__ float rs[4], rq[4];
-  __shared__ float sHst[2];
-  int b = blockIdx.x, tid = threadIdx.x, lane = tid & 63, wid = tid >> 6;
-  for (int i = tid*4; i < 8192; i += 1024)
+  __shared__ float P[20960];
+  float* sMT  = P;
+  float* sMN  = P + 8192;
+  float* sHn  = P + 16512;
+  float* sHOut= P + 17536;
+  float* sRk  = P + 18368;
+  float* sWk  = P + 18624;
+  float* sEv  = P + 18880;
+  float* sWs  = P + 19136;
+  float* sRw  = P + 19140;
+  float* sWw  = P + 19652;
+  float* sRc  = P + 20164;
+  float* sRcP = P + 20420;
+  float* rs   = P + 20932;
+  float* rq   = P + 20940;
+  float* sHst = P + 20948;
+  int b = blockIdx.x, tid = threadIdx.x, lane = tid & 63, wv = tid >> 6;
+  for (int i = tid*4; i < 8192; i += 2048)
     *(float4*)&sMT[i] = *(const float4*)&mem[(size_t)b*8192 + i];
-  {
-    const float* h0 = hp + (size_t)b*832;
-    const float* h1 = hp + 53248 + (size_t)b*832;
-    const float* h2 = hp + 2*53248 + (size_t)b*832;
-    const float* h3 = hp + 3*53248 + (size_t)b*832;
-    float v = h0[tid] + h1[tid] + h2[tid] + h3[tid] + b_rk[tid];
-    float ssum = wsum(v), ssq = wsum(v*v);
-    float mu = ssum*(1.f/64), var = ssq*(1.f/64) - mu*mu;
-    sRk[tid] = (v - mu)*rsqrtf(var+1e-5f)*rkn_g[lane] + rkn_b[lane];
-    v = h0[256+tid] + h1[256+tid] + h2[256+tid] + h3[256+tid] + b_wk[tid];
-    ssum = wsum(v); ssq = wsum(v*v);
-    mu = ssum*(1.f/64); var = ssq*(1.f/64) - mu*mu;
-    sWk[tid] = (v - mu)*rsqrtf(var+1e-5f)*wkn_g[lane] + wkn_b[lane];
-    sEv[tid] = sigm(h0[512+tid] + h1[512+tid] + h2[512+tid] + h3[512+tid] + b_ev[tid]);
-    if (tid < 4)
-      sWs[tid] = sigm(h0[768+tid] + h1[768+tid] + h2[768+tid] + h3[768+tid] + b_ws[tid]);
-  }
-  if (wid == 0) {
+  if (wv == 0) {
     float v0 = hstat[(b*64 + lane)*2], v1 = hstat[(b*64 + lane)*2 + 1];
     float s0 = wsum(v0), s1 = wsum(v1);
     if (lane == 0) {
@@ -602,16 +446,49 @@
     }
   }
   __syncthreads();
-  for (int r = wid; r < 128; r += 4) {
+  {
+    float mu = sHst[0], rstd = sHst[1];
+    for (int u = tid; u < 1024; u += 512)
+      sHn[u] = (hbuf[b*1024 + u] - mu)*rstd*cn_g[u] + cn_b[u];
+  }
+  for (int r = wv; r < 128; r += 8) {
     float v = sMT[r*64 + lane];
     float ssum = wsum(v), ssq = wsum(v*v);
     float mu = ssum*(1.f/64), var = ssq*(1.f/64) - mu*mu;
     sMN[r*65 + lane] = (v - mu)*rsqrtf(var+1e-5f)*mng[lane] + mnb[lane];
   }
   __syncthreads();
-#pragma unroll
-  for (int q = 0; q < 4; q++) {
-    int idx = tid + q*256;
+  for (int r = wv; r < 772; r += 8) {
+    const float* wr;
+    if (r < 256)      wr = W_rk + (size_t)r*1024;
+    else if (r < 512) wr = W_wk + (size_t)(r-256)*1024;
+    else if (r < 768) wr = W_ev + (size_t)(r-512)*1024;
+    else              wr = W_ws + (size_t)(r-768)*1024;
+    float acc = 0.f;
+#pragma unroll
+    for (int i = 0; i < 16; i++) acc += wr[lane + 64*i] * sHn[lane + 64*i];
+    acc = wsum(acc);
+    if (lane == 0) sHOut[r] = acc;
+  }
+  __syncthreads();
+  if (wv < 4) {
+    float v = sHOut[wv*64 + lane] + b_rk[wv*64 + lane];
+    float ssum = wsum(v), ssq = wsum(v*v);
+    float mu = ssum*(1.f/64), var = ssq*(1.f/64) - mu*mu;
+    sRk[wv*64 + lane] = (v - mu)*rsqrtf(var+1e-5f)*rkn_g[lane] + rkn_b[lane];
+  } else {
+    int n = wv - 4;
+    float v = sHOut[256 + n*64 + lane] + b_wk[n*64 + lane];
+    float ssum = wsum(v), ssq = wsum(v*v);
+    float mu = ssum*(1.f/64), var = ssq*(1.f/64) - mu*mu;
+    sWk[n*64 + lane] = (v - mu)*rsqrtf(var+1e-5f)*wkn_g[lane] + wkn_b[lane];
+  }
+  if (tid < 256) sEv[tid] = sigm(sHOut[512 + tid] + b_ev[tid]);
+  if (tid >= 256 && tid < 260) sWs[tid-256] = sigm(sHOut[768 + (tid-256)] + b_ws[tid-256]);
+  __syncthreads();
+#pragma unroll
+  for (int q = 0; q < 2; q++) {
+    int idx = tid + q*512;
     int which = idx >> 9;
     int n = (idx >> 7) & 3, m = idx & 127;
     const float* key = (which ? sWk : sRk) + n*64;
@@ -622,8 +499,8 @@
     (which ? sWw : sRw)[n*128 + m] = acc;
   }
   __syncthreads();
-  for (int r = wid; r < 8; r += 4) {
-    float* row = (r < 4) ? (sRw + r*128) : (sWw + (r-4)*128);
+  {
+    float* row = (wv < 4) ? (sRw + wv*128) : (sWw + (wv-4)*128);
     float a0 = row[lane], a1 = row[lane+64];
     float mx = fmaxf(a0, a1);
 #pragma unroll
@@ -634,13 +511,15 @@
   }
   __syncthreads();
   {
-    int n = tid >> 6, s2 = tid & 63;
+    int idx = tid & 255, h2 = tid >> 8;
+    int n = idx >> 6, s2 = idx & 63;
     float acc = 0.f;
-    for (int mm = 0; mm < 128; mm++) acc += sRw[n*128 + mm] * sMT[mm*64 + s2];
-    sRc[tid] = acc;
-  }
-  __syncthreads();
-  for (int idx = tid; idx < 8192; idx += 256) {
+    for (int mm = h2*64; mm < h2*64 + 64; mm++) acc += sRw[n*128 + mm] * sMT[mm*64 + s2];
+    sRcP[tid] = acc;
+  }
+  __syncthreads();
+  if (tid < 256) sRc[tid] = sRcP[tid] + sRcP[256 + tid];
+  for (int idx = tid; idx < 8192; idx += 512) {
     int mm = idx >> 6, s2 = idx & 63;
     float er = 0.f, ad = 0.f;
 #pragma unroll
@@ -651,50 +530,93 @@
     }
     float val = sMT[idx]*(1.0f - er) + ad;
     mem[(size_t)b*8192 + idx] = val;
-    storesplit(val, membH, membL, (size_t)b*8192 + idx);
-  }
-  float hmu = sHst[0], hrs = sHst[1];
-  float v5[5]; float s = 0.f, sq = 0.f;
-#pragma unroll
-  for (int i = 0; i < 5; i++) {
-    int k = tid + i*256;
-    float v = (k < 1024)
-      ? (hbuf[b*1024 + k] - hmu)*hrs*cn_g[k] + cn_b[k]
-      : sRc[k-1024];
-    v5[i] = v; s += v; sq += v*v;
-  }
-  s = wsum(s); sq = wsum(sq);
-  if (lane == 0) { rs[wid] = s; rq[wid] = sq; }
+    sMT[idx] = val;
+  }
+  __syncthreads();
+  short* sAH = (short*)(P + 8192);
+  short* sAL = sAH + 8192;
+  for (int idx = tid; idx < 8192; idx += 512) {
+    float v = sMT[idx];
+    short h = f2bf(v);
+    sAH[idx] = h;
+    sAL[idx] = f2bf(v - bf2f(h));
+  }
   __syncthreads();
   {
-    float ts = rs[0]+rs[1]+rs[2]+rs[3], tq = rq[0]+rq[1]+rq[2]+rq[3];
+    int ao = (wv*16 + (lane & 15))*64 + (lane >> 4)*8;
+    s8v ah0 = *(const s8v*)(sAH + ao);
+    s8v ah1 = *(const s8v*)(sAH + ao + 32);
+    s8v al0 = *(const s8v*)(sAL + ao);
+    s8v al1 = *(const s8v*)(sAL + ao + 32);
+    int bo = (lane & 15)*64 + (lane >> 4)*8;
+    for (int n = 0; n < 12; n++) {
+      s8v bh0 = *(const s8v*)(WqH + bo + n*1024);
+      s8v bh1 = *(const s8v*)(WqH + bo + n*1024 + 32);
+      s8v bl0 = *(const s8v*)(WqL + bo + n*1024);
+      s8v bl1 = *(const s8v*)(WqL + bo + n*1024 + 32);
+      f32x4 acc = {};
+      acc = __builtin_amdgcn_mfma_f32_16x16x32_bf16(ah0, bh0, acc, 0,0,0);
+      acc = __builtin_amdgcn_mfma_f32_16x16x32_bf16(ah1, bh1, acc, 0,0,0);
+      acc = __builtin_amdgcn_mfma_f32_16x16x32_bf16(al0, bh0, acc, 0,0,0);
+      acc = __builtin_amdgcn_mfma_f32_16x16x32_bf16(al1, bh1, acc, 0,0,0);
+      acc = __builtin_amdgcn_mfma_f32_16x16x32_bf16(ah0, bl0, acc, 0,0,0);
+      acc = __builtin_amdgcn_mfma_f32_16x16x32_bf16(ah1, bl1, acc, 0,0,0);
+      int j = n*16 + (lane & 15);
+      int ch = j >> 6, jj = j & 63;
+      float bv = attn_b[j];
+#pragma unroll
+      for (int r = 0; r < 4; r++) {
+        int m0 = wv*16 + (lane>>4)*4 + r;
+        qkv[((size_t)(b*3 + ch)*128 + m0)*64 + jj] = acc[r] + bv;
+      }
+    }
+  }
+  {
+    float v5[3]; float s = 0.f, sq = 0.f;
+#pragma unroll
+    for (int i = 0; i < 3; i++) {
+      int k = tid + i*512;
+      float v = 0.f;
+      if (k < 1280) v = (k < 1024) ? sHn[k] : sRc[k-1024];
+      v5[i] = v; s += v; sq += v*v;
+    }
+    s = wsum(s); sq = wsum(sq);
+    if (lane == 0) { rs[wv] = s; rq[wv] = sq; }
+    __syncthreads();
+    float ts = 0.f, tq = 0.f;
+#pragma unroll
+    for (int p = 0; p < 8; p++) { ts += rs[p]; tq += rq[p]; }
     float mu = ts/1280.f, var = tq/1280.f - mu*mu;
     float rstd = rsqrtf(var + 1e-5f);
 #pragma unroll
-    for (int i = 0; i < 5; i++) {
-      int k = tid + i*256;
-      pob16[b*1280 + k] = f2bf((v5[i] - mu)*rstd*pog[k] + pob[k]);
+    for (int i = 0; i < 3; i++) {
+      int k = tid + i*512;
+      if (k < 1280) pob16[b*1280 + k] = f2bf((v5[i] - mu)*rstd*pog[k] + pob[k]);
     }
   }
   if (tnext < 256) {
     __syncthreads();
-    float v3[3]; float s2 = 0.f, q2 = 0.f;
-#pragma unroll
-    for (int i = 0; i < 3; i++) {
-      int k = tid + i*256;
-      float v = (k < 512) ? x_emb[((size_t)b*256 + tnext)*512 + k] : sRc[k-512];
+    float v3[2]; float s2 = 0.f, q2 = 0.f;
+#pragma unroll
+    for (int i = 0; i < 2; i++) {
+      int k = tid + i*512;
+      float v = 0.f;
+      if (k < 768) v = (k < 512) ? x_emb[((size_t)b*256 + tnext)*512 + k] : sRc[k-512];
       v3[i] = v; s2 += v; q2 += v*v;
     }
     s2 = wsum(s2); q2 = wsum(q2);
-    if (lane == 0) { rs[wid] = s2; rq[wid] = q2; }
+    if (lane == 0) { rs[wv] = s2; rq[wv] = q2; }
     __syncthreads();
-    float ts = rs[0]+rs[1]+rs[2]+rs[3], tq = rq[0]+rq[1]+rq[2]+rq[3];
+    float ts = 0.f, tq = 0.f;
+#pragma unroll
+    for (int p = 0; p < 8; p++) { ts += rs[p]; tq += rq[p]; }
     float mu = ts/768.f, var = tq/768.f - mu*mu;
     float rstd = rsqrtf(var + 1e-5f);
 #pragma unroll
-    for (int i = 0; i < 3; i++) {
-      int k = tid + i*256;
-      storesplit((v3[i] - mu)*rstd*in_g[k] + in_b[k], inbHn, inbLn, b*1792 + k);
+    for (int i = 0; i < 2; i++) {
+      int k = tid + i*512;
+      if (k < 768)
+        storesplit((v3[i] - mu)*rstd*in_g[k] + in_b[k], inbHn, inbLn, b*1792 + k);
     }
   }
 }
@@ -754,62 +676,55 @@
   const float* b_proj = (const float*)d_in[38];
 
   float* ws = (float*)d_ws;
-  float* mem    = ws;
-  float* cbuf   = ws + 524288;
-  float* hbuf   = ws + 589824;
-  float* gatesP = ws + 655360;
-  float* hp     = ws + 1179648;
-  float* hstat  = ws + 1392640;
-  unsigned* tick = (unsigned*)(ws + 1400832);
-  float* qkvb   = ws + 1400896;
-  short* sb     = (short*)(ws + 2973760);
+  float* mem   = ws;
+  float* cbuf  = ws + 524288;
+  float* hbuf  = ws + 589824;
+  float* hstat = ws + 655360;
+  float* qkvb  = ws + 663552;
+  short* sb    = (short*)(ws + 2236416);
   short* inbH0 = sb;
   short* inbL0 = sb + 114688;
   short* inbH1 = sb + 229376;
   short* inbL1 = sb + 344064;
-  short* membH = sb + 458752;
-  short* membL = sb + 983040;
-  short* pob16 = sb + 1507328;
-  short* WgH   = sb + 1589248;
-  short* WgL   = sb + 8929280;
-  short* WhH   = sb + 16269312;
-  short* WhL   = sb + 17121280;
-  short* WqH   = sb + 17973248;
-  short* WqL   = sb + 17985536;
-  short* Wp16  = sb + 17997824;
+  short* pob16 = sb + 458752;
+  short* WqH   = sb + 540672;
+  short* WqL   = sb + 552960;
+  short* WgH   = sb + 565248;
+  short* WgL   = sb + 7905280;
+  short* Wp16  = sb + 15245312;
 
   hipMemsetAsync(ws, 0, 655360 * sizeof(float), stream);
-  hipMemsetAsync(tick, 0, 256, stream);
-  hipMemsetAsync(sb, 0, 1507328 * sizeof(short), stream);
+  hipMemsetAsync(sb, 0, 458752 * sizeof(short), stream);
 
   kprep_g<<<dim3(7, 4096), 256, 0, stream>>>(W_ih, W_hh, WgH, WgL);
   kprep_p<<<dim3(5, 1024), 256, 0, stream>>>(W_proj, Wp16);
-  kprep_h<<<dim3(4, 832), 256, 0, stream>>>(W_rk, W_wk, W_ev, W_ws, WhH, WhL);
   kprep_q<<<dim3(192), 64, 0, stream>>>(attn_w, WqH, WqL);
   k_prep0<<<64, 256, 0, stream>>>(x_emb, in_g, in_b, inbH0, inbL0);
+  k_prepq0<<<64, 256, 0, stream>>>(attn_b, qkvb);
 
   float* outs = (float*)d_out;
   short* bufsH[2] = {inbH0, inbH1};
   short* bufsL[2] = {inbL0, inbL1};
   for (int t = 0; t < 256; t++) {
-    kA<<<208, 256, 0, stream>>>(bufsH[t&1], bufsL[t&1], bufsH[(t+1)&1], bufsL[(t+1)&1],
-                                WgH, WgL, b_ih, b_hh, cbuf, hbuf, hstat, gatesP, tick,
-                                membH, membL, WqH, WqL, attn_b,
-                                pob16, Wp16, b_proj, qkvb, outs, t);
-    kB<<<308, 512, 0, stream>>>(mem, qkvb, attn_ow, attn_ob,
+    kA<<<200, 512, 0, stream>>>(bufsH[t&1], bufsL[t&1], bufsH[(t+1)&1], bufsL[(t+1)&1],
+                                WgH, WgL, b_ih, b_hh, cbuf, hbuf, hstat,
+                                qkvb, mem, attn_ow, attn_ob,
                                 l1_w, l1_b, l2_w, l2_b,
                                 tn1_g, tn1_b, tn2_g, tn2_b,
-                                hbuf, hstat, cn_g, cn_b, WhH, WhL, hp);
-    kC<<<64, 256, 0, stream>>>(mem, membH, membL, hp, hstat, hbuf,
+                                pob16, Wp16, b_proj, outs, t);
+    kC<<<64, 512, 0, stream>>>(mem, hstat, hbuf, cn_g, cn_b,
+                               W_rk, W_wk, W_ev, W_ws,
                                b_rk, b_wk, b_ev, b_ws,
-                               rkn_g, rkn_b, wkn_g, wkn_b, cn_g, cn_b,
+                               rkn_g, rkn_b, wkn_g, wkn_b,
                                mn_g, mn_b, po_g, po_b,
-                               x_emb, in_g, in_b,
-                               bufsH[(t+1)&1], bufsL[(t+1)&1], pob16, t+1);
-  }
-  kA<<<208, 256, 0, stream>>>(bufsH[0], bufsL[0], bufsH[1], bufsL[1],
-                              WgH, WgL, b_ih, b_hh, cbuf, hbuf, hstat, gatesP, tick,
-                              membH, membL, WqH, WqL, attn_b,
-                              pob16, Wp16, b_proj, qkvb, outs, 256);
+                               x_emb, in_g, in_b, WqH, WqL, attn_b,
+                               qkvb, bufsH[(t+1)&1], bufsL[(t+1)&1], pob16, t+1);
+  }
+  kA<<<200, 512, 0, stream>>>(bufsH[0], bufsL[0], bufsH[1], bufsL[1],
+                              WgH, WgL, b_ih, b_hh, cbuf, hbuf, hstat,
+                              qkvb, mem, attn_ow, attn_ob,
+                              l1_w, l1_b, l2_w, l2_b,
+                              tn1_g, tn1_b, tn2_g, tn2_b,
+                              pob16, Wp16, b_proj, outs, 256);
   k_final<<<2048, 256, 0, stream>>>(mem, hbuf, cbuf, (float*)d_out);
 }
```

New measurement: 52.32 ms. 91.2% more time.
